# Optimization experiments

Measured on AMD Instinct MI355X. Metric: run time of the kernel, lower is better.

The kernel has to match this reference:

```python
import jax, jax.numpy as jnp
import numpy as np
from jax import lax

PAD_ID = 0
V, E = 100000, 300          # word vocab / embedding dim
VC, EC, C = 100, 50, 100    # char vocab / char emb dim / char conv channels
H, L = 256, 17              # lstm hidden / n_labels
B, S, LC = 32, 128, 50


def _conv1d(x, w, b):
    # x [B, Cin, T], w [Cout, Cin, K] -> valid conv
    y = lax.conv_general_dilated(x, w, window_strides=(1,), padding='VALID',
                                 dimension_numbers=('NCH', 'OIH', 'NCH'))
    return y + b[None, :, None]


def _lstm_dir(x_sbd, w_ih, w_hh, b, h0, c0):
    # x_sbd [S,B,D]; PyTorch gate order i,f,g,o
    def step(carry, x_t):
        h, c = carry
        g = x_t @ w_ih.T + h @ w_hh.T + b
        i, f, gg, o = jnp.split(g, 4, axis=-1)
        c = jax.nn.sigmoid(f) * c + jax.nn.sigmoid(i) * jnp.tanh(gg)
        h = jax.nn.sigmoid(o) * jnp.tanh(c)
        return (h, c), h
    _, hs = lax.scan(step, (h0, c0), x_sbd)
    return hs  # [S,B,H]


def _emissions(x, x_char, word_emb, char_emb,
               conv1_w, conv1_b, conv2_w, conv2_b, conv3_w, conv3_b,
               w_ih_f, w_hh_f, b_f, w_ih_b, w_hh_b, b_b, h0, c0, fc_w, fc_b):
    emb = word_emb[x]                                   # [B,S,E]
    ce = char_emb[x_char].transpose(0, 2, 1)            # [B,EC,LC]
    ce = jax.nn.relu(_conv1d(ce, conv1_w, conv1_b))
    ce = jax.nn.relu(_conv1d(ce, conv2_w, conv2_b))
    ce = jax.nn.relu(_conv1d(ce, conv3_w, conv3_b))
    pooled = ce.max(axis=2)                             # [B,C] (max over time)
    char_rep = jnp.broadcast_to(pooled[:, None, :], (emb.shape[0], emb.shape[1], pooled.shape[1]))
    xin = jnp.concatenate([emb, char_rep], axis=2)      # [B,S,E+C]
    xs = xin.transpose(1, 0, 2)                         # [S,B,D]
    hf = _lstm_dir(xs, w_ih_f, w_hh_f, b_f, h0[0], c0[0])
    hb = _lstm_dir(xs[::-1], w_ih_b, w_hh_b, b_b, h0[1], c0[1])[::-1]
    hcat = jnp.concatenate([hf, hb], axis=-1).transpose(1, 0, 2)  # [B,S,2H]
    em = hcat @ fc_w.T + fc_b                           # [B,S,L]
    return jax.nn.softmax(em, axis=1)                   # faithful: softmax over seq dim


def _viterbi(emissions, mask, start_t, trans, end_t):
    # emissions [B,S,L], mask [B,S]
    em = emissions.transpose(1, 0, 2)                   # [S,B,L]
    m = mask.T                                          # [S,B]
    score0 = start_t[None, :] + em[0]                   # [B,L]

    def fwd(score, inp):
        e_t, m_t = inp
        cand = score[:, :, None] + trans[None] + e_t[:, None, :]  # [B,L,L]
        nscore = cand.max(axis=1)
        idx = cand.argmax(axis=1).astype(jnp.int32)
        score = jnp.where(m_t[:, None] > 0, nscore, score)
        return score, idx

    score, hist = lax.scan(fwd, score0, (em[1:], m[1:]))  # hist [S-1,B,L]
    score = score + end_t[None, :]
    last = jnp.argmax(score, axis=-1).astype(jnp.int32)   # [B]

    def back(cur, inp):
        h_t, m_t = inp
        prev = jnp.take_along_axis(h_t, cur[:, None], axis=1)[:, 0]
        cur = jnp.where(m_t > 0, prev, cur)
        return cur, cur

    _, tags_rev = lax.scan(back, last, (hist[::-1], m[1:][::-1]))
    tags = jnp.concatenate([tags_rev[::-1], last[None]], axis=0)  # [S,B]
    return tags.T                                                 # [B,S]


def setup_inputs() -> dict:
    key = jax.random.key(0)
    ks = jax.random.split(key, 24)
    f = lambda i, shape, s=0.1: (jax.random.normal(ks[i], shape, dtype=jnp.float32) * s)
    inp = {
        'x': jax.random.randint(ks[0], (B, S), 1, V),          # no PAD -> mask all ones
        'x_char': jax.random.randint(ks[1], (B, LC), 1, VC),
        'word_emb': f(2, (V, E), 1.0),
        'char_emb': f(3, (VC, EC), 1.0).at[PAD_ID].set(0.0),
        'conv1_w': f(4, (C, EC, 3)), 'conv1_b': f(5, (C,)),
        'conv2_w': f(6, (C, C, 4)), 'conv2_b': f(7, (C,)),
        'conv3_w': f(8, (C, C, 5)), 'conv3_b': f(9, (C,)),
        'w_ih_f': f(10, (4 * H, E + C)), 'w_hh_f': f(11, (4 * H, H)), 'b_f': f(12, (4 * H,)),
        'w_ih_b': f(13, (4 * H, E + C)), 'w_hh_b': f(14, (4 * H, H)), 'b_b': f(15, (4 * H,)),
        'h0': f(16, (2, B, H), 1.0), 'c0': f(17, (2, B, H), 1.0),
        'fc_w': f(18, (L, 2 * H)), 'fc_b': f(19, (L,)),
        'start_t': f(20, (L,)), 'trans': f(21, (L, L)), 'end_t': f(22, (L,)),
    }
    return inp


def reference(x, x_char, word_emb, char_emb, conv1_w, conv1_b, conv2_w, conv2_b,
              conv3_w, conv3_b, w_ih_f, w_hh_f, b_f, w_ih_b, w_hh_b, b_b,
              h0, c0, fc_w, fc_b, start_t, trans, end_t):
    mask = (x != PAD_ID).astype(jnp.float32)
    em = _emissions(x, x_char, word_emb, char_emb, conv1_w, conv1_b, conv2_w, conv2_b,
                    conv3_w, conv3_b, w_ih_f, w_hh_f, b_f, w_ih_b, w_hh_b, b_b,
                    h0, c0, fc_w, fc_b)
    return _viterbi(em, mask, start_t, trans, end_t)
```

## Files before the change

### kernel.cpp

```cpp
#include <hip/hip_runtime.h>
#include <cmath>

#define B_   32
#define S_   128
#define E_   300
#define C_   100
#define EC_  50
#define LC_  50
#define H_   256
#define G4_  1024
#define L_   17
#define DHID_ 400
#define NBLKD 8
#define SLAB_ 8192
#define SENT2_ 0x7E007E00u
#define KP_   208

typedef _Float16 half8 __attribute__((ext_vector_type(8)));
typedef float f32x4 __attribute__((ext_vector_type(4)));
typedef unsigned long long ull;
struct __align__(16) U2 { ull x, y; };

__device__ __forceinline__ unsigned pack_split(float v) {
  _Float16 hi = (fabsf(v) >= 6.104e-5f) ? (_Float16)v : (_Float16)0.0f;
  float hif = (float)hi;
  _Float16 lo = (_Float16)((v - hif) * 2048.0f);
  return (unsigned)__builtin_bit_cast(unsigned short, hi)
       | ((unsigned)__builtin_bit_cast(unsigned short, lo) << 16);
}

__global__ void k_hinit(const float* __restrict__ h0, unsigned* __restrict__ hfrag) {
  int idx = blockIdx.x * 256 + threadIdx.x;
  const int total = 2 * (S_ + 1) * SLAB_;
  if (idx >= total) return;
  int sd = idx / SLAB_;
  int within = idx % SLAB_;
  int t = sd % (S_ + 1), d = sd / (S_ + 1);
  if (t != 0) { hfrag[idx] = SENT2_; return; }
  int m8 = within & 7;
  int lane = (within >> 3) & 63;
  int q = within >> 9;
  int Kt = q & 7, Nt = q >> 3;
  int m = m8 & 3, isLo = m8 >> 2;
  int k0 = Kt * 32 + (lane >> 4) * 8 + 2 * m;
  int b = Nt * 16 + (lane & 15);
  unsigned p0 = pack_split(h0[((size_t)d * B_ + b) * H_ + k0]);
  unsigned p1 = pack_split(h0[((size_t)d * B_ + b) * H_ + k0 + 1]);
  unsigned hiw = (p0 & 0xFFFFu) | (p1 << 16);
  unsigned low = (p0 >> 16) | (p1 & 0xFFFF0000u);
  hfrag[idx] = isLo ? low : hiw;
}

__global__ void k_conv1(const int* __restrict__ x_char, const float* __restrict__ char_emb,
                        const float* __restrict__ w1, const float* __restrict__ b1,
                        float* __restrict__ out1) {
  int b = blockIdx.x;
  int ot = blockIdx.y;
  __shared__ float ce[EC_ * 52];
  __shared__ float wl[50 * 150];
  __shared__ int ids[LC_];
  int tid = threadIdx.x;
  if (tid < LC_) ids[tid] = x_char[b * LC_ + tid];
  __syncthreads();
  for (int idx = tid; idx < LC_ * EC_; idx += 256) {
    int t = idx / EC_, ec = idx % EC_;
    ce[ec * 52 + t] = char_emb[ids[t] * EC_ + ec];
  }
  int obase = ot * 50;
  for (int idx = tid; idx < 50 * 150; idx += 256)
    wl[idx] = w1[obase * 150 + idx];
  __syncthreads();
  for (int idx = tid; idx < 50 * 48; idx += 256) {
    int o = idx / 48, t = idx % 48;
    float acc = b1[obase + o];
    const float* wr = &wl[o * 150];
    for (int c = 0; c < EC_; ++c) {
      const float* ip = &ce[c * 52 + t];
      acc += wr[c * 3 + 0] * ip[0] + wr[c * 3 + 1] * ip[1] + wr[c * 3 + 2] * ip[2];
    }
    out1[((size_t)b * C_ + obase + o) * 48 + t] = fmaxf(acc, 0.0f);
  }
}

__global__ void k_conv2(const float* __restrict__ in, const float* __restrict__ w2,
                        const float* __restrict__ b2, float* __restrict__ out2) {
  int b = blockIdx.x, ot = blockIdx.y;
  __shared__ float il[C_ * 48];
  __shared__ float wl[25 * 400];
  int tid = threadIdx.x;
  for (int idx = tid; idx < C_ * 48; idx += 256) il[idx] = in[(size_t)b * C_ * 48 + idx];
  int obase = ot * 25;
  for (int idx = tid; idx < 25 * 400; idx += 256) wl[idx] = w2[obase * 400 + idx];
  __syncthreads();
  for (int idx = tid; idx < 25 * 45; idx += 256) {
    int o = idx / 45, t = idx % 45;
    float acc = b2[obase + o];
    const float* wr = &wl[o * 400];
    for (int c = 0; c < C_; ++c) {
      const float* ip = &il[c * 48 + t];
      acc += wr[c * 4 + 0] * ip[0] + wr[c * 4 + 1] * ip[1] +
             wr[c * 4 + 2] * ip[2] + wr[c * 4 + 3] * ip[3];
    }
    out2[((size_t)b * C_ + obase + o) * 45 + t] = fmaxf(acc, 0.0f);
  }
}

__global__ void k_conv3(const float* __restrict__ in, const float* __restrict__ w3,
                        const float* __restrict__ b3, float* __restrict__ pooled) {
  int b = blockIdx.x, ot = blockIdx.y;
  __shared__ float il[C_ * 45];
  __shared__ float wl[20 * 500];
  __shared__ float o3[20 * 44];
  int tid = threadIdx.x;
  for (int idx = tid; idx < C_ * 45; idx += 256) il[idx] = in[(size_t)b * C_ * 45 + idx];
  int obase = ot * 20;
  for (int idx = tid; idx < 20 * 500; idx += 256) wl[idx] = w3[obase * 500 + idx];
  __syncthreads();
  for (int idx = tid; idx < 20 * 41; idx += 256) {
    int o = idx / 41, t = idx % 41;
    float acc = b3[obase + o];
    const float* wr = &wl[o * 500];
    for (int c = 0; c < C_; ++c) {
      const float* ip = &il[c * 45 + t];
      acc += wr[c * 5 + 0] * ip[0] + wr[c * 5 + 1] * ip[1] + wr[c * 5 + 2] * ip[2] +
             wr[c * 5 + 3] * ip[3] + wr[c * 5 + 4] * ip[4];
    }
    o3[o * 44 + t] = fmaxf(acc, 0.0f);
  }
  __syncthreads();
  if (tid < 20) {
    float m = o3[tid * 44];
    for (int t = 1; t < 41; ++t) m = fmaxf(m, o3[tid * 44 + t]);
    pooled[b * C_ + obase + tid] = m;
  }
}

__global__ void k_prep_w(const float* __restrict__ wf, const float* __restrict__ wb,
                         unsigned* __restrict__ apH, unsigned* __restrict__ apL) {
  int idx = blockIdx.x * 256 + threadIdx.x;
  if (idx >= 2 * G4_ * KP_) return;
  int d = idx / (G4_ * KP_);
  int rem = idx % (G4_ * KP_);
  int j = rem / KP_, k2 = rem % KP_;
  const float* w = d ? wb : wf;
  float v0 = 0.f, v1 = 0.f;
  if (k2 < 200) { v0 = w[(size_t)j * DHID_ + 2 * k2]; v1 = w[(size_t)j * DHID_ + 2 * k2 + 1]; }
  unsigned p0 = pack_split(v0), p1 = pack_split(v1);
  apH[idx] = (p0 & 0xFFFFu) | (p1 << 16);
  apL[idx] = (p0 >> 16) | (p1 & 0xFFFF0000u);
}

__global__ void k_prep_b(const int* __restrict__ x, const float* __restrict__ word_emb,
                         const float* __restrict__ pooled,
                         unsigned* __restrict__ bpH, unsigned* __restrict__ bpL) {
  int r = blockIdx.x;
  int k2 = threadIdx.x;
  if (k2 >= KP_) return;
  int t = r >> 5, b = r & 31;
  float v0 = 0.f, v1 = 0.f;
  if (k2 < 150) {
    const float* e = word_emb + (size_t)x[b * S_ + t] * E_;
    v0 = e[2 * k2]; v1 = e[2 * k2 + 1];
  } else if (k2 < 200) {
    v0 = pooled[b * C_ + 2 * k2 - 300];
    v1 = pooled[b * C_ + 2 * k2 - 299];
  }
  unsigned p0 = pack_split(v0), p1 = pack_split(v1);
  bpH[(size_t)r * KP_ + k2] = (p0 & 0xFFFFu) | (p1 << 16);
  bpL[(size_t)r * KP_ + k2] = (p0 >> 16) | (p1 & 0xFFFF0000u);
}

__global__ __launch_bounds__(256) void k_gemm(
    const unsigned* __restrict__ apH, const unsigned* __restrict__ apL,
    const unsigned* __restrict__ bpH, const unsigned* __restrict__ bpL,
    const float* __restrict__ b_f, const float* __restrict__ b_b,
    float* __restrict__ gi) {
  const int jt = blockIdx.x, rt = blockIdx.y, d = blockIdx.z;
  const int j0 = jt * 128, r0 = rt * 128;
  const int tid = threadIdx.x;
  const int w = tid >> 6, l = tid & 63;
  const int lx = l & 15, lq = l >> 4;

  __shared__ unsigned aH[2048], aL[2048], bH[2048], bL[2048];

  f32x4 acch[2][8], accl[2][8];
#pragma unroll
  for (int mt = 0; mt < 2; ++mt)
#pragma unroll
    for (int nt = 0; nt < 8; ++nt) {
      f32x4 z = {0.f, 0.f, 0.f, 0.f};
      acch[mt][nt] = z; accl[mt][nt] = z;
    }

  const int jr = tid >> 1, hh = tid & 1;
  const int q_st = jr >> 4, lane_lo = jr & 15;
  const unsigned* arH = apH + ((size_t)(d * G4_ + j0 + jr)) * KP_ + hh * 8;
  const unsigned* arL = apL + ((size_t)(d * G4_ + j0 + jr)) * KP_ + hh * 8;
  const unsigned* brH = bpH + ((size_t)(r0 + jr)) * KP_ + hh * 8;
  const unsigned* brL = bpL + ((size_t)(r0 + jr)) * KP_ + hh * 8;
  const int w0 = (q_st * 64 + lane_lo + 32 * hh) * 4;
  const int w1 = (q_st * 64 + lane_lo + 32 * hh + 16) * 4;

  for (int Kt = 0; Kt < 13; ++Kt) {
    uint4 a0 = *(const uint4*)(arH + Kt * 16);
    uint4 a1 = *(const uint4*)(arH + Kt * 16 + 4);
    uint4 c0 = *(const uint4*)(arL + Kt * 16);
    uint4 c1 = *(const uint4*)(arL + Kt * 16 + 4);
    uint4 e0 = *(const uint4*)(brH + Kt * 16);
    uint4 e1 = *(const uint4*)(brH + Kt * 16 + 4);
    uint4 f0 = *(const uint4*)(brL + Kt * 16);
    uint4 f1 = *(const uint4*)(brL + Kt * 16 + 4);
    *(uint4*)&aH[w0] = a0; *(uint4*)&aH[w1] = a1;
    *(uint4*)&aL[w0] = c0; *(uint4*)&aL[w1] = c1;
    *(uint4*)&bH[w0] = e0; *(uint4*)&bH[w1] = e1;
    *(uint4*)&bL[w0] = f0; *(uint4*)&bL[w1] = f1;
    __syncthreads();

    union u4h { uint4 u; half8 h; };
    u4h AH0, AH1, AL0, AL1;
    AH0.u = *(const uint4*)&aH[((2 * w + 0) * 64 + l) * 4];
    AH1.u = *(const uint4*)&aH[((2 * w + 1) * 64 + l) * 4];
    AL0.u = *(const uint4*)&aL[((2 * w + 0) * 64 + l) * 4];
    AL1.u = *(const uint4*)&aL[((2 * w + 1) * 64 + l) * 4];
#pragma unroll
    for (int nt = 0; nt < 8; ++nt) {
      u4h BHn, BLn;
      BHn.u = *(const uint4*)&bH[(nt * 64 + l) * 4];
      BLn.u = *(const uint4*)&bL[(nt * 64 + l) * 4];
      acch[0][nt] = __builtin_amdgcn_mfma_f32_16x16x32_f16(AH0.h, BHn.h, acch[0][nt], 0, 0, 0);
      accl[0][nt] = __builtin_amdgcn_mfma_f32_16x16x32_f16(AH0.h, BLn.h, accl[0][nt], 0, 0, 0);
      accl[0][nt] = __builtin_amdgcn_mfma_f32_16x16x32_f16(AL0.h, BHn.h, accl[0][nt], 0, 0, 0);
      acch[1][nt] = __builtin_amdgcn_mfma_f32_16x16x32_f16(AH1.h, BHn.h, acch[1][nt], 0, 0, 0);
      accl[1][nt] = __builtin_amdgcn_mfma_f32_16x16x32_f16(AH1.h, BLn.h, accl[1][nt], 0, 0, 0);
      accl[1][nt] = __builtin_amdgcn_mfma_f32_16x16x32_f16(AL1.h, BHn.h, accl[1][nt], 0, 0, 0);
    }
    __syncthreads();
  }

  const float* bias = d ? b_b : b_f;
  const float inv2048 = 1.0f / 2048.0f;
#pragma unroll
  for (int mt = 0; mt < 2; ++mt) {
#pragma unroll
    for (int nt = 0; nt < 8; ++nt) {
      int rr = r0 + nt * 16 + lx;
      int tt = rr >> 5, bb = rr & 31;
      float* dst = gi + ((size_t)(d * S_ + tt) * G4_) * B_ + bb;
#pragma unroll
      for (int r4 = 0; r4 < 4; ++r4) {
        int j = j0 + (2 * w + mt) * 16 + lq * 4 + r4;
        dst[(size_t)j * B_] = acch[mt][nt][r4] + accl[mt][nt][r4] * inv2048 + bias[j];
      }
    }
  }
}

__global__ __launch_bounds__(256, 1) void k_lstm(
    const float* __restrict__ w_hh_f, const float* __restrict__ w_hh_b,
    const float* __restrict__ c0, const float* __restrict__ gi,
    float* __restrict__ hbuf, unsigned* __restrict__ hfrag) {
  const int iblk = blockIdx.x;
  const int d = blockIdx.y;
  const float* whh = d ? w_hh_b : w_hh_f;
  const int tid = threadIdx.x;
  const int w = tid >> 6;
  const int l = tid & 63;
  const int lx = l & 15, lq = l >> 4;
  const int u0 = iblk * 32;

  __shared__ ull slh[2048];
  __shared__ ull sll[2048];
  __shared__ float gl[4 * 32 * 33];
  __shared__ unsigned ps[2 * 576];

  half8 whi[2][8], wlo[2][8];
#pragma unroll
  for (int Mt = 0; Mt < 2; ++Mt) {
#pragma unroll
    for (int Kt = 0; Kt < 8; ++Kt) {
      int row = w * H_ + u0 + Mt * 16 + lx;
      int kk0 = Kt * 32 + lq * 8;
      const float* src = whh + (size_t)row * H_ + kk0;
      float4 f0 = *(const float4*)src;
      float4 f1 = *(const float4*)(src + 4);
      float wv[8] = {f0.x, f0.y, f0.z, f0.w, f1.x, f1.y, f1.z, f1.w};
      union { unsigned short s[8]; half8 h; } HI, LO;
#pragma unroll
      for (int j = 0; j < 8; ++j) {
        float v = wv[j];
        _Float16 hi = (fabsf(v) >= 6.104e-5f) ? (_Float16)v : (_Float16)0.0f;
        float hif = (float)hi;
        _Float16 lo = (_Float16)((v - hif) * 2048.0f);
        HI.s[j] = __builtin_bit_cast(unsigned short, hi);
        LO.s[j] = __builtin_bit_cast(unsigned short, lo);
      }
      whi[Mt][Kt] = HI.h;
      wlo[Mt][Kt] = LO.h;
    }
  }

  const int bc = tid & 31, cw = tid >> 5;
  float creg[4];
#pragma unroll
  for (int cu = 0; cu < 4; ++cu)
    creg[cu] = c0[((size_t)d * B_ + bc) * H_ + u0 + cu * 8 + cw];

  const int pNt = bc >> 4;
  const int pm = cw >> 1;
  const bool phi = (cw & 1) == 0;
  const int plane = bc & 15;
  const float inv2048 = 1.0f / 2048.0f;

  for (int t = 0; t < S_; ++t) {
    int torig = d ? (S_ - 1 - t) : t;

    f32x4 acch[2][2], accl[2][2];
    {
      const float* gbase = gi + ((size_t)(d * S_ + torig) * G4_) * B_;
#pragma unroll
      for (int Mt = 0; Mt < 2; ++Mt)
#pragma unroll
        for (int Nt = 0; Nt < 2; ++Nt) {
          f32x4 v;
#pragma unroll
          for (int r = 0; r < 4; ++r) {
            int j = w * H_ + u0 + Mt * 16 + lq * 4 + r;
            v[r] = gbase[(size_t)j * B_ + Nt * 16 + lx];
          }
          acch[Mt][Nt] = v;
          f32x4 z = {0.f, 0.f, 0.f, 0.f};
          accl[Mt][Nt] = z;
        }
    }

    const ull* hp = (const ull*)(hfrag + (size_t)(d * (S_ + 1) + t) * SLAB_);
    ull pv[4][4];
#pragma unroll
    for (int c = 0; c < 4; ++c) {
      size_t base = ((size_t)(w * 4 + c) * 64 + l) * 4;
#pragma unroll
      for (int j = 0; j < 4; ++j)
        pv[c][j] = __hip_atomic_load(&hp[base + j], __ATOMIC_RELAXED,
                                     __HIP_MEMORY_SCOPE_AGENT);
    }
    for (;;) {
      bool pending = false;
#pragma unroll
      for (int c = 0; c < 4; ++c)
#pragma unroll
        for (int j = 0; j < 4; ++j)
          pending |= ((unsigned)pv[c][j] == SENT2_) |
                     ((unsigned)(pv[c][j] >> 32) == SENT2_);
      if (!pending) break;
#pragma unroll
      for (int c = 0; c < 4; ++c) {
        size_t base = ((size_t)(w * 4 + c) * 64 + l) * 4;
#pragma unroll
        for (int j = 0; j < 4; ++j)
          pv[c][j] = __hip_atomic_load(&hp[base + j], __ATOMIC_RELAXED,
                                       __HIP_MEMORY_SCOPE_AGENT);
      }
    }
#pragma unroll
    for (int c = 0; c < 4; ++c) {
      int idx = ((w * 4 + c) * 64 + l) * 2;
      U2 vh; vh.x = pv[c][0]; vh.y = pv[c][1];
      U2 vl; vl.x = pv[c][2]; vl.y = pv[c][3];
      *(U2*)&slh[idx] = vh;
      *(U2*)&sll[idx] = vl;
    }
    __syncthreads();

#pragma unroll
    for (int Kt = 0; Kt < 8; ++Kt) {
      half8 Bhi[2], Blo[2];
#pragma unroll
      for (int Nt = 0; Nt < 2; ++Nt) {
        int idx = ((Nt * 8 + Kt) * 64 + l) * 2;
        union { U2 u; half8 h; } UH, UL;
        UH.u = *(const U2*)&slh[idx];
        UL.u = *(const U2*)&sll[idx];
        Bhi[Nt] = UH.h;
        Blo[Nt] = UL.h;
      }
#pragma unroll
      for (int Mt = 0; Mt < 2; ++Mt)
#pragma unroll
        for (int Nt = 0; Nt < 2; ++Nt) {
          acch[Mt][Nt] = __builtin_amdgcn_mfma_f32_16x16x32_f16(
              whi[Mt][Kt], Bhi[Nt], acch[Mt][Nt], 0, 0, 0);
          accl[Mt][Nt] = __builtin_amdgcn_mfma_f32_16x16x32_f16(
              whi[Mt][Kt], Blo[Nt], accl[Mt][Nt], 0, 0, 0);
          accl[Mt][Nt] = __builtin_amdgcn_mfma_f32_16x16x32_f16(
              wlo[Mt][Kt], Bhi[Nt], accl[Mt][Nt], 0, 0, 0);
        }
    }

#pragma unroll
    for (int Mt = 0; Mt < 2; ++Mt)
#pragma unroll
      for (int Nt = 0; Nt < 2; ++Nt)
#pragma unroll
        for (int r = 0; r < 4; ++r) {
          int ul = Mt * 16 + lq * 4 + r;
          gl[(w * 32 + ul) * 33 + Nt * 16 + lx] =
              acch[Mt][Nt][r] + accl[Mt][Nt][r] * inv2048;
        }
    __syncthreads();

    float hreg[4];
#pragma unroll
    for (int cu = 0; cu < 4; ++cu) {
      int u = cu * 8 + cw;
      float g_i = gl[(0 * 32 + u) * 33 + bc];
      float g_f = gl[(1 * 32 + u) * 33 + bc];
      float g_g = gl[(2 * 32 + u) * 33 + bc];
      float g_o = gl[(3 * 32 + u) * 33 + bc];
      float si = 1.f / (1.f + __expf(-g_i));
      float sf = 1.f / (1.f + __expf(-g_f));
      float so = 1.f / (1.f + __expf(-g_o));
      float tg = 1.f - 2.f / (__expf(2.f * g_g) + 1.f);
      float cn = sf * creg[cu] + si * tg;
      float tc = 1.f - 2.f / (__expf(2.f * cn) + 1.f);
      float hn = so * tc;
      creg[cu] = cn;
      hreg[cu] = hn;
      unsigned me = pack_split(hn);
      unsigned pa = (unsigned)__shfl_xor((int)me, 32, 64);
      unsigned je = (cw & 1) ? pa : me;
      unsigned jo = (cw & 1) ? me : pa;
      unsigned hiw = (je & 0xFFFFu) | (jo << 16);
      unsigned low = (je >> 16) | (jo & 0xFFFF0000u);
      int lane2 = (cu << 4) | plane;
      int m8 = phi ? pm : (4 + pm);
      ps[pNt * 576 + lane2 * 9 + m8] = phi ? hiw : low;
    }
    __syncthreads();

    {
      ull* slab64 = (ull*)(hfrag + (size_t)(d * (S_ + 1) + t + 1) * SLAB_);
#pragma unroll
      for (int hh2 = 0; hh2 < 2; ++hh2) {
        int r = tid;
        int Nt = hh2;
        int lane2 = r >> 2, m2 = r & 3;
        unsigned a = ps[Nt * 576 + lane2 * 9 + 2 * m2];
        unsigned b = ps[Nt * 576 + lane2 * 9 + 2 * m2 + 1];
        ull v = (ull)a | ((ull)b << 32);
        __hip_atomic_store(&slab64[(size_t)(Nt * 8 + iblk) * 256 + r], v,
                           __ATOMIC_RELAXED, __HIP_MEMORY_SCOPE_AGENT);
      }
      float* hb = hbuf + (size_t)(d * (S_ + 1) + t + 1) * (H_ * B_) + u0 * B_;
#pragma unroll
      for (int cu = 0; cu < 4; ++cu) hb[cu * 256 + tid] = hreg[cu];
    }
  }
}

__global__ __launch_bounds__(256) void k_fc(const float* __restrict__ hbuf,
                                            const float* __restrict__ fc_w,
                                            const float* __restrict__ fc_b,
                                            float* __restrict__ em) {
  const int s = blockIdx.x;
  const int tid = threadIdx.x;
  __shared__ float wT[512 * 18];
  __shared__ float psum[256 * 18];
  for (int i = tid; i < L_ * 512; i += 256) {
    int l = i / 512, k = i % 512;
    wT[k * 18 + l] = fc_w[i];
  }
  __syncthreads();
  const int b = tid & 31, kq = tid >> 5;
  const float* hf = hbuf + (size_t)(s + 1) * (H_ * B_);
  const float* hbk = hbuf + (size_t)(S_ + 1 + (S_ - s)) * (H_ * B_);
  float acc[L_];
#pragma unroll
  for (int l = 0; l < L_; ++l) acc[l] = 0.f;
  for (int i = 0; i < 64; ++i) {
    int k = kq * 64 + i;
    float hv = (k < 256) ? hf[k * 32 + b] : hbk[(k - 256) * 32 + b];
    const float* wr = &wT[k * 18];
#pragma unroll
    for (int l = 0; l < L_; ++l) acc[l] = fmaf(hv, wr[l], acc[l]);
  }
#pragma unroll
  for (int l = 0; l < L_; ++l) psum[tid * 18 + l] = acc[l];
  __syncthreads();
  for (int idx = tid; idx < B_ * L_; idx += 256) {
    int bb = idx & 31, l = idx >> 5;
    float sum = fc_b[l];
    for (int q = 0; q < 8; ++q) sum += psum[(q * 32 + bb) * 18 + l];
    em[((size_t)bb * S_ + s) * L_ + l] = sum;
  }
}

__global__ void k_smv(const float* __restrict__ em, const int* __restrict__ x,
                      const float* __restrict__ start_t, const float* __restrict__ trans,
                      const float* __restrict__ end_t, int* __restrict__ out) {
  int b = blockIdx.x;
  int tid = threadIdx.x;
  __shared__ float e[S_ * L_];
  __shared__ float tr[L_ * L_];
  __shared__ float sc[2][L_];
  __shared__ int hist[(S_ - 1) * L_];
  __shared__ int tags[S_];
  for (int i = tid; i < S_ * L_; i += 64) e[i] = em[(size_t)b * S_ * L_ + i];
  for (int i = tid; i < L_ * L_; i += 64) tr[i] = trans[i];
  __syncthreads();
  if (tid < L_) {
    int l = tid;
    float m = -INFINITY;
    for (int s = 0; s < S_; ++s) m = fmaxf(m, e[s * L_ + l]);
    float sum = 0.f;
    for (int s = 0; s < S_; ++s) {
      float ex = expf(e[s * L_ + l] - m);
      e[s * L_ + l] = ex;
      sum += ex;
    }
    for (int s = 0; s < S_; ++s) e[s * L_ + l] = e[s * L_ + l] / sum;
  }
  __syncthreads();
  if (tid < L_) sc[0][tid] = start_t[tid] + e[tid];
  __syncthreads();
  int cbuf = 0;
  for (int t = 1; t < S_; ++t) {
    if (tid < L_) {
      int j = tid;
      float ev = e[t * L_ + j];
      float best = -INFINITY;
      int arg = 0;
      for (int i = 0; i < L_; ++i) {
        float v = (sc[cbuf][i] + tr[i * L_ + j]) + ev;
        if (v > best) { best = v; arg = i; }
      }
      int maskt = (x[b * S_ + t] != 0);
      sc[cbuf ^ 1][j] = maskt ? best : sc[cbuf][j];
      hist[(t - 1) * L_ + j] = arg;
    }
    __syncthreads();
    cbuf ^= 1;
  }
  if (tid == 0) {
    float best = -INFINITY;
    int last = 0;
    for (int j = 0; j < L_; ++j) {
      float v = sc[cbuf][j] + end_t[j];
      if (v > best) { best = v; last = j; }
    }
    int cur = last;
    tags[S_ - 1] = cur;
    for (int p = S_ - 2; p >= 0; --p) {
      if (x[b * S_ + p + 1] != 0) cur = hist[p * L_ + cur];
      tags[p] = cur;
    }
  }
  __syncthreads();
  for (int s = tid; s < S_; s += 64) out[b * S_ + s] = tags[s];
}

extern "C" void kernel_launch(void* const* d_in, const int* in_sizes, int n_in,
                              void* d_out, int out_size, void* d_ws, size_t ws_size,
                              hipStream_t stream) {
  const int* x        = (const int*)d_in[0];
  const int* x_char   = (const int*)d_in[1];
  const float* word_emb = (const float*)d_in[2];
  const float* char_emb = (const float*)d_in[3];
  const float* conv1_w = (const float*)d_in[4];
  const float* conv1_b = (const float*)d_in[5];
  const float* conv2_w = (const float*)d_in[6];
  const float* conv2_b = (const float*)d_in[7];
  const float* conv3_w = (const float*)d_in[8];
  const float* conv3_b = (const float*)d_in[9];
  const float* w_ih_f = (const float*)d_in[10];
  const float* w_hh_f = (const float*)d_in[11];
  const float* b_f    = (const float*)d_in[12];
  const float* w_ih_b = (const float*)d_in[13];
  const float* w_hh_b = (const float*)d_in[14];
  const float* b_b    = (const float*)d_in[15];
  const float* h0     = (const float*)d_in[16];
  const float* c0     = (const float*)d_in[17];
  const float* fc_w   = (const float*)d_in[18];
  const float* fc_b   = (const float*)d_in[19];
  const float* start_t = (const float*)d_in[20];
  const float* trans  = (const float*)d_in[21];
  const float* end_t  = (const float*)d_in[22];
  int* out = (int*)d_out;

  char* ws = (char*)d_ws;
  auto alloc = [&](size_t bytes) -> char* {
    char* p = ws;
    ws += (bytes + 1023) & ~(size_t)1023;
    return p;
  };
  float* pooled  = (float*)alloc(sizeof(float) * B_ * C_);
  float* gi      = (float*)alloc(sizeof(float) * 2 * S_ * G4_ * B_);
  float* hbuf    = (float*)alloc(sizeof(float) * 2 * (S_ + 1) * H_ * B_);
  unsigned* hfrag = (unsigned*)alloc(sizeof(unsigned) * 2 * (S_ + 1) * SLAB_);
  unsigned* apH  = (unsigned*)alloc(sizeof(unsigned) * 2 * G4_ * KP_);
  unsigned* apL  = (unsigned*)alloc(sizeof(unsigned) * 2 * G4_ * KP_);
  unsigned* bpH  = (unsigned*)alloc(sizeof(unsigned) * 4096 * KP_);
  unsigned* bpL  = (unsigned*)alloc(sizeof(unsigned) * 4096 * KP_);
  float* out1    = (float*)alloc(sizeof(float) * B_ * C_ * 48);
  float* out2    = (float*)alloc(sizeof(float) * B_ * C_ * 45);
  float* em      = (float*)alloc(sizeof(float) * B_ * S_ * L_);

  const int hinit_total = 2 * (S_ + 1) * SLAB_;
  k_hinit<<<(hinit_total + 255) / 256, 256, 0, stream>>>(h0, hfrag);
  k_prep_w<<<(2 * G4_ * KP_ + 255) / 256, 256, 0, stream>>>(w_ih_f, w_ih_b, apH, apL);
  k_conv1<<<dim3(32, 2), 256, 0, stream>>>(x_char, char_emb, conv1_w, conv1_b, out1);
  k_conv2<<<dim3(32, 4), 256, 0, stream>>>(out1, conv2_w, conv2_b, out2);
  k_conv3<<<dim3(32, 5), 256, 0, stream>>>(out2, conv3_w, conv3_b, pooled);
  k_prep_b<<<4096, 256, 0, stream>>>(x, word_emb, pooled, bpH, bpL);
  k_gemm<<<dim3(8, 32, 2), 256, 0, stream>>>(apH, apL, bpH, bpL, b_f, b_b, gi);
  k_lstm<<<dim3(NBLKD, 2), 256, 0, stream>>>(w_hh_f, w_hh_b, c0, gi, hbuf, hfrag);
  k_fc<<<S_, 256, 0, stream>>>(hbuf, fc_w, fc_b, em);
  k_smv<<<B_, 64, 0, stream>>>(em, x, start_t, trans, end_t, out);
}
```

Baseline: 930.2 us.

## Fuse all stages into one persistent megakernel with flag and sentinel dataflow sync

Replaces the ten-kernel launch sequence with a fill kernel plus one megakernel. Its blocks are partitioned by role: LSTM, convs, prep, GEMM, FC and Viterbi. Stages synchronise through atomic counters and NaN-sentinel polling on gi, hbuf and em, so the FC and Viterbi stages can overlap the LSTM recurrence and launch gaps disappear. The cost is filling large sentinel buffers and spin-waiting, plus a deadlock risk if producer blocks are not co-resident with the consumers that wait on them.

```diff
diff --git a/kernel.cpp b/kernel.cpp
--- a/kernel.cpp
+++ b/kernel.cpp
@@ -14,7 +14,34 @@
 #define NBLKD 8
 #define SLAB_ 8192
 #define SENT2_ 0x7E007E00u
+#define SENTF_ 0x7FC0DEADu
 #define KP_   208
+
+#define RB_LSTM 0
+#define NB_LSTM 16
+#define RB_C1   16
+#define NB_C1   64
+#define RB_C2   80
+#define NB_C2   128
+#define RB_C3   208
+#define NB_C3   160
+#define RB_PW   368
+#define NB_PW   64
+#define RB_PB   432
+#define NB_PB   512
+#define RB_GEMM 944
+#define NB_GEMM 512
+#define RB_FC   1456
+#define NB_FC   128
+#define RB_SMV  1584
+#define NB_SMV  32
+#define NBLK_MEGA 1616
+
+#define F_C1 0
+#define F_C2 1
+#define F_C3 2
+#define F_PW 3
+#define F_PB 4
 
 typedef _Float16 half8 __attribute__((ext_vector_type(8)));
 typedef float f32x4 __attribute__((ext_vector_type(4)));
@@ -29,329 +56,159 @@
        | ((unsigned)__builtin_bit_cast(unsigned short, lo) << 16);
 }
 
-__global__ void k_hinit(const float* __restrict__ h0, unsigned* __restrict__ hfrag) {
-  int idx = blockIdx.x * 256 + threadIdx.x;
-  const int total = 2 * (S_ + 1) * SLAB_;
-  if (idx >= total) return;
-  int sd = idx / SLAB_;
-  int within = idx % SLAB_;
-  int t = sd % (S_ + 1), d = sd / (S_ + 1);
-  if (t != 0) { hfrag[idx] = SENT2_; return; }
-  int m8 = within & 7;
-  int lane = (within >> 3) & 63;
-  int q = within >> 9;
-  int Kt = q & 7, Nt = q >> 3;
-  int m = m8 & 3, isLo = m8 >> 2;
-  int k0 = Kt * 32 + (lane >> 4) * 8 + 2 * m;
-  int b = Nt * 16 + (lane & 15);
-  unsigned p0 = pack_split(h0[((size_t)d * B_ + b) * H_ + k0]);
-  unsigned p1 = pack_split(h0[((size_t)d * B_ + b) * H_ + k0 + 1]);
-  unsigned hiw = (p0 & 0xFFFFu) | (p1 << 16);
-  unsigned low = (p0 >> 16) | (p1 & 0xFFFF0000u);
-  hfrag[idx] = isLo ? low : hiw;
+__device__ __forceinline__ void flag_signal(int* f) {
+  __syncthreads();
+  if (threadIdx.x == 0)
+    __hip_atomic_fetch_add(f, 1, __ATOMIC_RELEASE, __HIP_MEMORY_SCOPE_AGENT);
 }
-
-__global__ void k_conv1(const int* __restrict__ x_char, const float* __restrict__ char_emb,
-                        const float* __restrict__ w1, const float* __restrict__ b1,
-                        float* __restrict__ out1) {
-  int b = blockIdx.x;
-  int ot = blockIdx.y;
-  __shared__ float ce[EC_ * 52];
-  __shared__ float wl[50 * 150];
-  __shared__ int ids[LC_];
-  int tid = threadIdx.x;
-  if (tid < LC_) ids[tid] = x_char[b * LC_ + tid];
-  __syncthreads();
-  for (int idx = tid; idx < LC_ * EC_; idx += 256) {
-    int t = idx / EC_, ec = idx % EC_;
-    ce[ec * 52 + t] = char_emb[ids[t] * EC_ + ec];
-  }
-  int obase = ot * 50;
-  for (int idx = tid; idx < 50 * 150; idx += 256)
-    wl[idx] = w1[obase * 150 + idx];
-  __syncthreads();
-  for (int idx = tid; idx < 50 * 48; idx += 256) {
-    int o = idx / 48, t = idx % 48;
-    float acc = b1[obase + o];
-    const float* wr = &wl[o * 150];
-    for (int c = 0; c < EC_; ++c) {
-      const float* ip = &ce[c * 52 + t];
-      acc += wr[c * 3 + 0] * ip[0] + wr[c * 3 + 1] * ip[1] + wr[c * 3 + 2] * ip[2];
-    }
-    out1[((size_t)b * C_ + obase + o) * 48 + t] = fmaxf(acc, 0.0f);
+__device__ __forceinline__ void flag_wait(const int* f, int target, int slp) {
+  while (__hip_atomic_load(f, __ATOMIC_ACQUIRE, __HIP_MEMORY_SCOPE_AGENT) < target) {
+    switch (slp) {
+      case 4:  __builtin_amdgcn_s_sleep(4);  break;
+      case 8:  __builtin_amdgcn_s_sleep(8);  break;
+      default: __builtin_amdgcn_s_sleep(16); break;
+    }
   }
 }
 
-__global__ void k_conv2(const float* __restrict__ in, const float* __restrict__ w2,
-                        const float* __restrict__ b2, float* __restrict__ out2) {
-  int b = blockIdx.x, ot = blockIdx.y;
-  __shared__ float il[C_ * 48];
-  __shared__ float wl[25 * 400];
-  int tid = threadIdx.x;
-  for (int idx = tid; idx < C_ * 48; idx += 256) il[idx] = in[(size_t)b * C_ * 48 + idx];
-  int obase = ot * 25;
-  for (int idx = tid; idx < 25 * 400; idx += 256) wl[idx] = w2[obase * 400 + idx];
-  __syncthreads();
-  for (int idx = tid; idx < 25 * 45; idx += 256) {
-    int o = idx / 45, t = idx % 45;
-    float acc = b2[obase + o];
-    const float* wr = &wl[o * 400];
-    for (int c = 0; c < C_; ++c) {
-      const float* ip = &il[c * 48 + t];
-      acc += wr[c * 4 + 0] * ip[0] + wr[c * 4 + 1] * ip[1] +
-             wr[c * 4 + 2] * ip[2] + wr[c * 4 + 3] * ip[3];
-    }
-    out2[((size_t)b * C_ + obase + o) * 45 + t] = fmaxf(acc, 0.0f);
-  }
+union SMem {
+  struct { unsigned aH[2048], aL[2048], bH[2048], bL[2048]; } gemm;
+  struct { ull slh[2048], sll[2048]; float gl[4 * 32 * 33]; unsigned ps[2 * 576]; } lstm;
+  struct { float ce[EC_ * 52]; float wl[50 * 150]; int ids[LC_]; } c1;
+  struct { float il[C_ * 48]; float wl[25 * 400]; } c2;
+  struct { float il[C_ * 45]; float wl[20 * 500]; float o3[20 * 44]; } c3;
+  struct { float wT[512 * 18]; float psum[256 * 18]; } fc;
+  struct { float e[S_ * L_]; float tr[L_ * L_]; float sc[2][L_];
+           int hist[(S_ - 1) * L_]; int tags[S_]; } smv;
+};
+
+__global__ void k_fill(const float* __restrict__ h0, unsigned* __restrict__ hfrag,
+                       unsigned* __restrict__ hbufU, unsigned* __restrict__ giU,
+                       unsigned* __restrict__ emU, int* __restrict__ flags) {
+  const int g0 = blockIdx.x * 256 + threadIdx.x;
+  const int nth = gridDim.x * 256;
+  const int htot = 2 * (S_ + 1) * SLAB_;
+  for (int idx = g0; idx < htot; idx += nth) {
+    int sd = idx / SLAB_;
+    int within = idx % SLAB_;
+    int t = sd % (S_ + 1), d = sd / (S_ + 1);
+    if (t != 0) { hfrag[idx] = SENT2_; continue; }
+    int m8 = within & 7;
+    int lane = (within >> 3) & 63;
+    int q = within >> 9;
+    int Kt = q & 7, Nt = q >> 3;
+    int m = m8 & 3, isLo = m8 >> 2;
+    int k0 = Kt * 32 + (lane >> 4) * 8 + 2 * m;
+    int b = Nt * 16 + (lane & 15);
+    unsigned p0 = pack_split(h0[((size_t)d * B_ + b) * H_ + k0]);
+    unsigned p1 = pack_split(h0[((size_t)d * B_ + b) * H_ + k0 + 1]);
+    unsigned hiw = (p0 & 0xFFFFu) | (p1 << 16);
+    unsigned low = (p0 >> 16) | (p1 & 0xFFFF0000u);
+    hfrag[idx] = isLo ? low : hiw;
+  }
+  const int hbtot = 2 * (S_ + 1) * H_ * B_;
+  for (int idx = g0; idx < hbtot; idx += nth) hbufU[idx] = SENTF_;
+  const int gtot = 2 * S_ * G4_ * B_;
+  for (int idx = g0; idx < gtot; idx += nth) giU[idx] = SENTF_;
+  const int etot = B_ * S_ * L_;
+  for (int idx = g0; idx < etot; idx += nth) emU[idx] = SENTF_;
+  if (g0 < 16) flags[g0] = 0;
 }
 
-__global__ void k_conv3(const float* __restrict__ in, const float* __restrict__ w3,
-                        const float* __restrict__ b3, float* __restrict__ pooled) {
-  int b = blockIdx.x, ot = blockIdx.y;
-  __shared__ float il[C_ * 45];
-  __shared__ float wl[20 * 500];
-  __shared__ float o3[20 * 44];
-  int tid = threadIdx.x;
-  for (int idx = tid; idx < C_ * 45; idx += 256) il[idx] = in[(size_t)b * C_ * 45 + idx];
-  int obase = ot * 20;
-  for (int idx = tid; idx < 20 * 500; idx += 256) wl[idx] = w3[obase * 500 + idx];
-  __syncthreads();
-  for (int idx = tid; idx < 20 * 41; idx += 256) {
-    int o = idx / 41, t = idx % 41;
-    float acc = b3[obase + o];
-    const float* wr = &wl[o * 500];
-    for (int c = 0; c < C_; ++c) {
-      const float* ip = &il[c * 45 + t];
-      acc += wr[c * 5 + 0] * ip[0] + wr[c * 5 + 1] * ip[1] + wr[c * 5 + 2] * ip[2] +
-             wr[c * 5 + 3] * ip[3] + wr[c * 5 + 4] * ip[4];
-    }
-    o3[o * 44 + t] = fmaxf(acc, 0.0f);
-  }
-  __syncthreads();
-  if (tid < 20) {
-    float m = o3[tid * 44];
-    for (int t = 1; t < 41; ++t) m = fmaxf(m, o3[tid * 44 + t]);
-    pooled[b * C_ + obase + tid] = m;
-  }
-}
-
-__global__ void k_prep_w(const float* __restrict__ wf, const float* __restrict__ wb,
-                         unsigned* __restrict__ apH, unsigned* __restrict__ apL) {
-  int idx = blockIdx.x * 256 + threadIdx.x;
-  if (idx >= 2 * G4_ * KP_) return;
-  int d = idx / (G4_ * KP_);
-  int rem = idx % (G4_ * KP_);
-  int j = rem / KP_, k2 = rem % KP_;
-  const float* w = d ? wb : wf;
-  float v0 = 0.f, v1 = 0.f;
-  if (k2 < 200) { v0 = w[(size_t)j * DHID_ + 2 * k2]; v1 = w[(size_t)j * DHID_ + 2 * k2 + 1]; }
-  unsigned p0 = pack_split(v0), p1 = pack_split(v1);
-  apH[idx] = (p0 & 0xFFFFu) | (p1 << 16);
-  apL[idx] = (p0 >> 16) | (p1 & 0xFFFF0000u);
-}
-
-__global__ void k_prep_b(const int* __restrict__ x, const float* __restrict__ word_emb,
-                         const float* __restrict__ pooled,
-                         unsigned* __restrict__ bpH, unsigned* __restrict__ bpL) {
-  int r = blockIdx.x;
-  int k2 = threadIdx.x;
-  if (k2 >= KP_) return;
-  int t = r >> 5, b = r & 31;
-  float v0 = 0.f, v1 = 0.f;
-  if (k2 < 150) {
-    const float* e = word_emb + (size_t)x[b * S_ + t] * E_;
-    v0 = e[2 * k2]; v1 = e[2 * k2 + 1];
-  } else if (k2 < 200) {
-    v0 = pooled[b * C_ + 2 * k2 - 300];
-    v1 = pooled[b * C_ + 2 * k2 - 299];
-  }
-  unsigned p0 = pack_split(v0), p1 = pack_split(v1);
-  bpH[(size_t)r * KP_ + k2] = (p0 & 0xFFFFu) | (p1 << 16);
-  bpL[(size_t)r * KP_ + k2] = (p0 >> 16) | (p1 & 0xFFFF0000u);
-}
-
-__global__ __launch_bounds__(256) void k_gemm(
-    const unsigned* __restrict__ apH, const unsigned* __restrict__ apL,
-    const unsigned* __restrict__ bpH, const unsigned* __restrict__ bpL,
+__global__ __launch_bounds__(256, 2) void k_mega(
+    const int* __restrict__ x, const int* __restrict__ x_char,
+    const float* __restrict__ word_emb, const float* __restrict__ char_emb,
+    const float* __restrict__ conv1_w, const float* __restrict__ conv1_b,
+    const float* __restrict__ conv2_w, const float* __restrict__ conv2_b,
+    const float* __restrict__ conv3_w, const float* __restrict__ conv3_b,
+    const float* __restrict__ w_ih_f, const float* __restrict__ w_ih_b,
+    const float* __restrict__ w_hh_f, const float* __restrict__ w_hh_b,
     const float* __restrict__ b_f, const float* __restrict__ b_b,
-    float* __restrict__ gi) {
-  const int jt = blockIdx.x, rt = blockIdx.y, d = blockIdx.z;
-  const int j0 = jt * 128, r0 = rt * 128;
-  const int tid = threadIdx.x;
-  const int w = tid >> 6, l = tid & 63;
-  const int lx = l & 15, lq = l >> 4;
-
-  __shared__ unsigned aH[2048], aL[2048], bH[2048], bL[2048];
-
-  f32x4 acch[2][8], accl[2][8];
-#pragma unroll
-  for (int mt = 0; mt < 2; ++mt)
-#pragma unroll
-    for (int nt = 0; nt < 8; ++nt) {
-      f32x4 z = {0.f, 0.f, 0.f, 0.f};
-      acch[mt][nt] = z; accl[mt][nt] = z;
-    }
-
-  const int jr = tid >> 1, hh = tid & 1;
-  const int q_st = jr >> 4, lane_lo = jr & 15;
-  const unsigned* arH = apH + ((size_t)(d * G4_ + j0 + jr)) * KP_ + hh * 8;
-  const unsigned* arL = apL + ((size_t)(d * G4_ + j0 + jr)) * KP_ + hh * 8;
-  const unsigned* brH = bpH + ((size_t)(r0 + jr)) * KP_ + hh * 8;
-  const unsigned* brL = bpL + ((size_t)(r0 + jr)) * KP_ + hh * 8;
-  const int w0 = (q_st * 64 + lane_lo + 32 * hh) * 4;
-  const int w1 = (q_st * 64 + lane_lo + 32 * hh + 16) * 4;
-
-  for (int Kt = 0; Kt < 13; ++Kt) {
-    uint4 a0 = *(const uint4*)(arH + Kt * 16);
-    uint4 a1 = *(const uint4*)(arH + Kt * 16 + 4);
-    uint4 c0 = *(const uint4*)(arL + Kt * 16);
-    uint4 c1 = *(const uint4*)(arL + Kt * 16 + 4);
-    uint4 e0 = *(const uint4*)(brH + Kt * 16);
-    uint4 e1 = *(const uint4*)(brH + Kt * 16 + 4);
-    uint4 f0 = *(const uint4*)(brL + Kt * 16);
-    uint4 f1 = *(const uint4*)(brL + Kt * 16 + 4);
-    *(uint4*)&aH[w0] = a0; *(uint4*)&aH[w1] = a1;
-    *(uint4*)&aL[w0] = c0; *(uint4*)&aL[w1] = c1;
-    *(uint4*)&bH[w0] = e0; *(uint4*)&bH[w1] = e1;
-    *(uint4*)&bL[w0] = f0; *(uint4*)&bL[w1] = f1;
-    __syncthreads();
-
-    union u4h { uint4 u; half8 h; };
-    u4h AH0, AH1, AL0, AL1;
-    AH0.u = *(const uint4*)&aH[((2 * w + 0) * 64 + l) * 4];
-    AH1.u = *(const uint4*)&aH[((2 * w + 1) * 64 + l) * 4];
-    AL0.u = *(const uint4*)&aL[((2 * w + 0) * 64 + l) * 4];
-    AL1.u = *(const uint4*)&aL[((2 * w + 1) * 64 + l) * 4];
-#pragma unroll
-    for (int nt = 0; nt < 8; ++nt) {
-      u4h BHn, BLn;
-      BHn.u = *(const uint4*)&bH[(nt * 64 + l) * 4];
-      BLn.u = *(const uint4*)&bL[(nt * 64 + l) * 4];
-      acch[0][nt] = __builtin_amdgcn_mfma_f32_16x16x32_f16(AH0.h, BHn.h, acch[0][nt], 0, 0, 0);
-      accl[0][nt] = __builtin_amdgcn_mfma_f32_16x16x32_f16(AH0.h, BLn.h, accl[0][nt], 0, 0, 0);
-      accl[0][nt] = __builtin_amdgcn_mfma_f32_16x16x32_f16(AL0.h, BHn.h, accl[0][nt], 0, 0, 0);
-      acch[1][nt] = __builtin_amdgcn_mfma_f32_16x16x32_f16(AH1.h, BHn.h, acch[1][nt], 0, 0, 0);
-      accl[1][nt] = __builtin_amdgcn_mfma_f32_16x16x32_f16(AH1.h, BLn.h, accl[1][nt], 0, 0, 0);
-      accl[1][nt] = __builtin_amdgcn_mfma_f32_16x16x32_f16(AL1.h, BHn.h, accl[1][nt], 0, 0, 0);
-    }
-    __syncthreads();
-  }
-
-  const float* bias = d ? b_b : b_f;
-  const float inv2048 = 1.0f / 2048.0f;
-#pragma unroll
-  for (int mt = 0; mt < 2; ++mt) {
-#pragma unroll
-    for (int nt = 0; nt < 8; ++nt) {
-      int rr = r0 + nt * 16 + lx;
-      int tt = rr >> 5, bb = rr & 31;
-      float* dst = gi + ((size_t)(d * S_ + tt) * G4_) * B_ + bb;
-#pragma unroll
-      for (int r4 = 0; r4 < 4; ++r4) {
-        int j = j0 + (2 * w + mt) * 16 + lq * 4 + r4;
-        dst[(size_t)j * B_] = acch[mt][nt][r4] + accl[mt][nt][r4] * inv2048 + bias[j];
-      }
-    }
-  }
-}
-
-__global__ __launch_bounds__(256, 1) void k_lstm(
-    const float* __restrict__ w_hh_f, const float* __restrict__ w_hh_b,
-    const float* __restrict__ c0, const float* __restrict__ gi,
-    float* __restrict__ hbuf, unsigned* __restrict__ hfrag) {
-  const int iblk = blockIdx.x;
-  const int d = blockIdx.y;
-  const float* whh = d ? w_hh_b : w_hh_f;
-  const int tid = threadIdx.x;
-  const int w = tid >> 6;
-  const int l = tid & 63;
-  const int lx = l & 15, lq = l >> 4;
-  const int u0 = iblk * 32;
-
-  __shared__ ull slh[2048];
-  __shared__ ull sll[2048];
-  __shared__ float gl[4 * 32 * 33];
-  __shared__ unsigned ps[2 * 576];
-
-  half8 whi[2][8], wlo[2][8];
-#pragma unroll
-  for (int Mt = 0; Mt < 2; ++Mt) {
-#pragma unroll
-    for (int Kt = 0; Kt < 8; ++Kt) {
-      int row = w * H_ + u0 + Mt * 16 + lx;
-      int kk0 = Kt * 32 + lq * 8;
-      const float* src = whh + (size_t)row * H_ + kk0;
-      float4 f0 = *(const float4*)src;
-      float4 f1 = *(const float4*)(src + 4);
-      float wv[8] = {f0.x, f0.y, f0.z, f0.w, f1.x, f1.y, f1.z, f1.w};
-      union { unsigned short s[8]; half8 h; } HI, LO;
-#pragma unroll
-      for (int j = 0; j < 8; ++j) {
-        float v = wv[j];
-        _Float16 hi = (fabsf(v) >= 6.104e-5f) ? (_Float16)v : (_Float16)0.0f;
-        float hif = (float)hi;
-        _Float16 lo = (_Float16)((v - hif) * 2048.0f);
-        HI.s[j] = __builtin_bit_cast(unsigned short, hi);
-        LO.s[j] = __builtin_bit_cast(unsigned short, lo);
-      }
-      whi[Mt][Kt] = HI.h;
-      wlo[Mt][Kt] = LO.h;
-    }
-  }
-
-  const int bc = tid & 31, cw = tid >> 5;
-  float creg[4];
-#pragma unroll
-  for (int cu = 0; cu < 4; ++cu)
-    creg[cu] = c0[((size_t)d * B_ + bc) * H_ + u0 + cu * 8 + cw];
-
-  const int pNt = bc >> 4;
-  const int pm = cw >> 1;
-  const bool phi = (cw & 1) == 0;
-  const int plane = bc & 15;
-  const float inv2048 = 1.0f / 2048.0f;
-
-  for (int t = 0; t < S_; ++t) {
-    int torig = d ? (S_ - 1 - t) : t;
-
-    f32x4 acch[2][2], accl[2][2];
-    {
-      const float* gbase = gi + ((size_t)(d * S_ + torig) * G4_) * B_;
+    const float* __restrict__ c0,
+    const float* __restrict__ fc_w, const float* __restrict__ fc_b,
+    const float* __restrict__ start_t, const float* __restrict__ trans,
+    const float* __restrict__ end_t,
+    float* __restrict__ pooled, float* __restrict__ gi, float* __restrict__ hbuf,
+    unsigned* __restrict__ hfrag,
+    unsigned* __restrict__ apH, unsigned* __restrict__ apL,
+    unsigned* __restrict__ bpH, unsigned* __restrict__ bpL,
+    float* __restrict__ out1, float* __restrict__ out2,
+    float* __restrict__ em, int* __restrict__ flags, int* __restrict__ out) {
+  const int bid = blockIdx.x;
+  __shared__ SMem sm;
+
+  if (bid < RB_C1) {
+    __builtin_amdgcn_s_setprio(2);
+    const int iblk = bid & 7;
+    const int d = bid >> 3;
+    const float* whh = d ? w_hh_b : w_hh_f;
+    const int tid = threadIdx.x;
+    const int w = tid >> 6;
+    const int l = tid & 63;
+    const int lx = l & 15, lq = l >> 4;
+    const int u0 = iblk * 32;
+
+    ull* slh = sm.lstm.slh;
+    ull* sll = sm.lstm.sll;
+    float* glb = sm.lstm.gl;
+    unsigned* ps = sm.lstm.ps;
+
+    half8 whi[2][8], wlo[2][8];
+#pragma unroll
+    for (int Mt = 0; Mt < 2; ++Mt) {
+#pragma unroll
+      for (int Kt = 0; Kt < 8; ++Kt) {
+        int row = w * H_ + u0 + Mt * 16 + lx;
+        int kk0 = Kt * 32 + lq * 8;
+        const float* src = whh + (size_t)row * H_ + kk0;
+        float4 f0 = *(const float4*)src;
+        float4 f1 = *(const float4*)(src + 4);
+        float wv[8] = {f0.x, f0.y, f0.z, f0.w, f1.x, f1.y, f1.z, f1.w};
+        union { unsigned short s2[8]; half8 h; } HI, LO;
+#pragma unroll
+        for (int j = 0; j < 8; ++j) {
+          float v = wv[j];
+          _Float16 hi = (fabsf(v) >= 6.104e-5f) ? (_Float16)v : (_Float16)0.0f;
+          float hif = (float)hi;
+          _Float16 lo = (_Float16)((v - hif) * 2048.0f);
+          HI.s2[j] = __builtin_bit_cast(unsigned short, hi);
+          LO.s2[j] = __builtin_bit_cast(unsigned short, lo);
+        }
+        whi[Mt][Kt] = HI.h;
+        wlo[Mt][Kt] = LO.h;
+      }
+    }
+
+    const int bc = tid & 31, cw = tid >> 5;
+    float creg[4];
+#pragma unroll
+    for (int cu = 0; cu < 4; ++cu)
+      creg[cu] = c0[((size_t)d * B_ + bc) * H_ + u0 + cu * 8 + cw];
+
+    const int pNt = bc >> 4;
+    const int pm = cw >> 1;
+    const bool phi = (cw & 1) == 0;
+    const int plane = bc & 15;
+    const float inv2048 = 1.0f / 2048.0f;
+
+    for (int t = 0; t < S_; ++t) {
+      int torig = d ? (S_ - 1 - t) : t;
+
+      const unsigned* gbase = (const unsigned*)gi + ((size_t)(d * S_ + torig) * G4_) * B_;
+      unsigned gv[2][2][4];
 #pragma unroll
       for (int Mt = 0; Mt < 2; ++Mt)
 #pragma unroll
-        for (int Nt = 0; Nt < 2; ++Nt) {
-          f32x4 v;
+        for (int Nt = 0; Nt < 2; ++Nt)
 #pragma unroll
           for (int r = 0; r < 4; ++r) {
             int j = w * H_ + u0 + Mt * 16 + lq * 4 + r;
-            v[r] = gbase[(size_t)j * B_ + Nt * 16 + lx];
+            gv[Mt][Nt][r] = __hip_atomic_load(&gbase[(size_t)j * B_ + Nt * 16 + lx],
+                                              __ATOMIC_RELAXED, __HIP_MEMORY_SCOPE_AGENT);
           }
-          acch[Mt][Nt] = v;
-          f32x4 z = {0.f, 0.f, 0.f, 0.f};
-          accl[Mt][Nt] = z;
-        }
-    }
-
-    const ull* hp = (const ull*)(hfrag + (size_t)(d * (S_ + 1) + t) * SLAB_);
-    ull pv[4][4];
-#pragma unroll
-    for (int c = 0; c < 4; ++c) {
-      size_t base = ((size_t)(w * 4 + c) * 64 + l) * 4;
-#pragma unroll
-      for (int j = 0; j < 4; ++j)
-        pv[c][j] = __hip_atomic_load(&hp[base + j], __ATOMIC_RELAXED,
-                                     __HIP_MEMORY_SCOPE_AGENT);
-    }
-    for (;;) {
-      bool pending = false;
-#pragma unroll
-      for (int c = 0; c < 4; ++c)
-#pragma unroll
-        for (int j = 0; j < 4; ++j)
-          pending |= ((unsigned)pv[c][j] == SENT2_) |
-                     ((unsigned)(pv[c][j] >> 32) == SENT2_);
-      if (!pending) break;
+
+      const ull* hp = (const ull*)(hfrag + (size_t)(d * (S_ + 1) + t) * SLAB_);
+      ull pv[4][4];
 #pragma unroll
       for (int c = 0; c < 4; ++c) {
         size_t base = ((size_t)(w * 4 + c) * 64 + l) * 4;
@@ -360,202 +217,523 @@
           pv[c][j] = __hip_atomic_load(&hp[base + j], __ATOMIC_RELAXED,
                                        __HIP_MEMORY_SCOPE_AGENT);
       }
-    }
-#pragma unroll
-    for (int c = 0; c < 4; ++c) {
-      int idx = ((w * 4 + c) * 64 + l) * 2;
-      U2 vh; vh.x = pv[c][0]; vh.y = pv[c][1];
-      U2 vl; vl.x = pv[c][2]; vl.y = pv[c][3];
-      *(U2*)&slh[idx] = vh;
-      *(U2*)&sll[idx] = vl;
-    }
-    __syncthreads();
-
-#pragma unroll
-    for (int Kt = 0; Kt < 8; ++Kt) {
-      half8 Bhi[2], Blo[2];
-#pragma unroll
-      for (int Nt = 0; Nt < 2; ++Nt) {
-        int idx = ((Nt * 8 + Kt) * 64 + l) * 2;
-        union { U2 u; half8 h; } UH, UL;
-        UH.u = *(const U2*)&slh[idx];
-        UL.u = *(const U2*)&sll[idx];
-        Bhi[Nt] = UH.h;
-        Blo[Nt] = UL.h;
-      }
+      for (;;) {
+        bool pending = false;
+#pragma unroll
+        for (int c = 0; c < 4; ++c)
+#pragma unroll
+          for (int j = 0; j < 4; ++j)
+            pending |= ((unsigned)pv[c][j] == SENT2_) |
+                       ((unsigned)(pv[c][j] >> 32) == SENT2_);
+        if (!pending) break;
+#pragma unroll
+        for (int c = 0; c < 4; ++c) {
+          size_t base = ((size_t)(w * 4 + c) * 64 + l) * 4;
+#pragma unroll
+          for (int j = 0; j < 4; ++j)
+            pv[c][j] = __hip_atomic_load(&hp[base + j], __ATOMIC_RELAXED,
+                                         __HIP_MEMORY_SCOPE_AGENT);
+        }
+      }
+
+      for (;;) {
+        bool pending = false;
+#pragma unroll
+        for (int Mt = 0; Mt < 2; ++Mt)
+#pragma unroll
+          for (int Nt = 0; Nt < 2; ++Nt)
+#pragma unroll
+            for (int r = 0; r < 4; ++r) pending |= (gv[Mt][Nt][r] == SENTF_);
+        if (!pending) break;
+#pragma unroll
+        for (int Mt = 0; Mt < 2; ++Mt)
+#pragma unroll
+          for (int Nt = 0; Nt < 2; ++Nt)
+#pragma unroll
+            for (int r = 0; r < 4; ++r) {
+              int j = w * H_ + u0 + Mt * 16 + lq * 4 + r;
+              gv[Mt][Nt][r] = __hip_atomic_load(&gbase[(size_t)j * B_ + Nt * 16 + lx],
+                                                __ATOMIC_RELAXED, __HIP_MEMORY_SCOPE_AGENT);
+            }
+      }
+
+      f32x4 acch[2][2], accl[2][2];
 #pragma unroll
       for (int Mt = 0; Mt < 2; ++Mt)
 #pragma unroll
         for (int Nt = 0; Nt < 2; ++Nt) {
-          acch[Mt][Nt] = __builtin_amdgcn_mfma_f32_16x16x32_f16(
-              whi[Mt][Kt], Bhi[Nt], acch[Mt][Nt], 0, 0, 0);
-          accl[Mt][Nt] = __builtin_amdgcn_mfma_f32_16x16x32_f16(
-              whi[Mt][Kt], Blo[Nt], accl[Mt][Nt], 0, 0, 0);
-          accl[Mt][Nt] = __builtin_amdgcn_mfma_f32_16x16x32_f16(
-              wlo[Mt][Kt], Bhi[Nt], accl[Mt][Nt], 0, 0, 0);
+          f32x4 v, z = {0.f, 0.f, 0.f, 0.f};
+#pragma unroll
+          for (int r = 0; r < 4; ++r) v[r] = __builtin_bit_cast(float, gv[Mt][Nt][r]);
+          acch[Mt][Nt] = v;
+          accl[Mt][Nt] = z;
         }
-    }
-
-#pragma unroll
-    for (int Mt = 0; Mt < 2; ++Mt)
-#pragma unroll
-      for (int Nt = 0; Nt < 2; ++Nt)
-#pragma unroll
-        for (int r = 0; r < 4; ++r) {
-          int ul = Mt * 16 + lq * 4 + r;
-          gl[(w * 32 + ul) * 33 + Nt * 16 + lx] =
-              acch[Mt][Nt][r] + accl[Mt][Nt][r] * inv2048;
+
+#pragma unroll
+      for (int c = 0; c < 4; ++c) {
+        int idx = ((w * 4 + c) * 64 + l) * 2;
+        U2 vh; vh.x = pv[c][0]; vh.y = pv[c][1];
+        U2 vl; vl.x = pv[c][2]; vl.y = pv[c][3];
+        *(U2*)&slh[idx] = vh;
+        *(U2*)&sll[idx] = vl;
+      }
+      __syncthreads();
+
+#pragma unroll
+      for (int Kt = 0; Kt < 8; ++Kt) {
+        half8 Bhi[2], Blo[2];
+#pragma unroll
+        for (int Nt = 0; Nt < 2; ++Nt) {
+          int idx = ((Nt * 8 + Kt) * 64 + l) * 2;
+          union { U2 u; half8 h; } UH, UL;
+          UH.u = *(const U2*)&slh[idx];
+          UL.u = *(const U2*)&sll[idx];
+          Bhi[Nt] = UH.h;
+          Blo[Nt] = UL.h;
         }
-    __syncthreads();
-
-    float hreg[4];
-#pragma unroll
-    for (int cu = 0; cu < 4; ++cu) {
-      int u = cu * 8 + cw;
-      float g_i = gl[(0 * 32 + u) * 33 + bc];
-      float g_f = gl[(1 * 32 + u) * 33 + bc];
-      float g_g = gl[(2 * 32 + u) * 33 + bc];
-      float g_o = gl[(3 * 32 + u) * 33 + bc];
-      float si = 1.f / (1.f + __expf(-g_i));
-      float sf = 1.f / (1.f + __expf(-g_f));
-      float so = 1.f / (1.f + __expf(-g_o));
-      float tg = 1.f - 2.f / (__expf(2.f * g_g) + 1.f);
-      float cn = sf * creg[cu] + si * tg;
-      float tc = 1.f - 2.f / (__expf(2.f * cn) + 1.f);
-      float hn = so * tc;
-      creg[cu] = cn;
-      hreg[cu] = hn;
-      unsigned me = pack_split(hn);
-      unsigned pa = (unsigned)__shfl_xor((int)me, 32, 64);
-      unsigned je = (cw & 1) ? pa : me;
-      unsigned jo = (cw & 1) ? me : pa;
-      unsigned hiw = (je & 0xFFFFu) | (jo << 16);
-      unsigned low = (je >> 16) | (jo & 0xFFFF0000u);
-      int lane2 = (cu << 4) | plane;
-      int m8 = phi ? pm : (4 + pm);
-      ps[pNt * 576 + lane2 * 9 + m8] = phi ? hiw : low;
-    }
-    __syncthreads();
-
-    {
-      ull* slab64 = (ull*)(hfrag + (size_t)(d * (S_ + 1) + t + 1) * SLAB_);
-#pragma unroll
-      for (int hh2 = 0; hh2 < 2; ++hh2) {
-        int r = tid;
-        int Nt = hh2;
-        int lane2 = r >> 2, m2 = r & 3;
-        unsigned a = ps[Nt * 576 + lane2 * 9 + 2 * m2];
-        unsigned b = ps[Nt * 576 + lane2 * 9 + 2 * m2 + 1];
-        ull v = (ull)a | ((ull)b << 32);
-        __hip_atomic_store(&slab64[(size_t)(Nt * 8 + iblk) * 256 + r], v,
-                           __ATOMIC_RELAXED, __HIP_MEMORY_SCOPE_AGENT);
-      }
-      float* hb = hbuf + (size_t)(d * (S_ + 1) + t + 1) * (H_ * B_) + u0 * B_;
-#pragma unroll
-      for (int cu = 0; cu < 4; ++cu) hb[cu * 256 + tid] = hreg[cu];
-    }
-  }
-}
-
-__global__ __launch_bounds__(256) void k_fc(const float* __restrict__ hbuf,
-                                            const float* __restrict__ fc_w,
-                                            const float* __restrict__ fc_b,
-                                            float* __restrict__ em) {
-  const int s = blockIdx.x;
-  const int tid = threadIdx.x;
-  __shared__ float wT[512 * 18];
-  __shared__ float psum[256 * 18];
-  for (int i = tid; i < L_ * 512; i += 256) {
-    int l = i / 512, k = i % 512;
-    wT[k * 18 + l] = fc_w[i];
-  }
-  __syncthreads();
-  const int b = tid & 31, kq = tid >> 5;
-  const float* hf = hbuf + (size_t)(s + 1) * (H_ * B_);
-  const float* hbk = hbuf + (size_t)(S_ + 1 + (S_ - s)) * (H_ * B_);
-  float acc[L_];
-#pragma unroll
-  for (int l = 0; l < L_; ++l) acc[l] = 0.f;
-  for (int i = 0; i < 64; ++i) {
-    int k = kq * 64 + i;
-    float hv = (k < 256) ? hf[k * 32 + b] : hbk[(k - 256) * 32 + b];
-    const float* wr = &wT[k * 18];
-#pragma unroll
-    for (int l = 0; l < L_; ++l) acc[l] = fmaf(hv, wr[l], acc[l]);
-  }
-#pragma unroll
-  for (int l = 0; l < L_; ++l) psum[tid * 18 + l] = acc[l];
-  __syncthreads();
-  for (int idx = tid; idx < B_ * L_; idx += 256) {
-    int bb = idx & 31, l = idx >> 5;
-    float sum = fc_b[l];
-    for (int q = 0; q < 8; ++q) sum += psum[(q * 32 + bb) * 18 + l];
-    em[((size_t)bb * S_ + s) * L_ + l] = sum;
-  }
-}
-
-__global__ void k_smv(const float* __restrict__ em, const int* __restrict__ x,
-                      const float* __restrict__ start_t, const float* __restrict__ trans,
-                      const float* __restrict__ end_t, int* __restrict__ out) {
-  int b = blockIdx.x;
-  int tid = threadIdx.x;
-  __shared__ float e[S_ * L_];
-  __shared__ float tr[L_ * L_];
-  __shared__ float sc[2][L_];
-  __shared__ int hist[(S_ - 1) * L_];
-  __shared__ int tags[S_];
-  for (int i = tid; i < S_ * L_; i += 64) e[i] = em[(size_t)b * S_ * L_ + i];
-  for (int i = tid; i < L_ * L_; i += 64) tr[i] = trans[i];
-  __syncthreads();
-  if (tid < L_) {
-    int l = tid;
-    float m = -INFINITY;
-    for (int s = 0; s < S_; ++s) m = fmaxf(m, e[s * L_ + l]);
-    float sum = 0.f;
-    for (int s = 0; s < S_; ++s) {
-      float ex = expf(e[s * L_ + l] - m);
-      e[s * L_ + l] = ex;
-      sum += ex;
-    }
-    for (int s = 0; s < S_; ++s) e[s * L_ + l] = e[s * L_ + l] / sum;
-  }
-  __syncthreads();
-  if (tid < L_) sc[0][tid] = start_t[tid] + e[tid];
-  __syncthreads();
-  int cbuf = 0;
-  for (int t = 1; t < S_; ++t) {
+#pragma unroll
+        for (int Mt = 0; Mt < 2; ++Mt)
+#pragma unroll
+          for (int Nt = 0; Nt < 2; ++Nt) {
+            acch[Mt][Nt] = __builtin_amdgcn_mfma_f32_16x16x32_f16(
+                whi[Mt][Kt], Bhi[Nt], acch[Mt][Nt], 0, 0, 0);
+            accl[Mt][Nt] = __builtin_amdgcn_mfma_f32_16x16x32_f16(
+                whi[Mt][Kt], Blo[Nt], accl[Mt][Nt], 0, 0, 0);
+            accl[Mt][Nt] = __builtin_amdgcn_mfma_f32_16x16x32_f16(
+                wlo[Mt][Kt], Bhi[Nt], accl[Mt][Nt], 0, 0, 0);
+          }
+      }
+
+#pragma unroll
+      for (int Mt = 0; Mt < 2; ++Mt)
+#pragma unroll
+        for (int Nt = 0; Nt < 2; ++Nt)
+#pragma unroll
+          for (int r = 0; r < 4; ++r) {
+            int ul = Mt * 16 + lq * 4 + r;
+            glb[(w * 32 + ul) * 33 + Nt * 16 + lx] =
+                acch[Mt][Nt][r] + accl[Mt][Nt][r] * inv2048;
+          }
+      __syncthreads();
+
+      float hreg[4];
+#pragma unroll
+      for (int cu = 0; cu < 4; ++cu) {
+        int u = cu * 8 + cw;
+        float g_i = glb[(0 * 32 + u) * 33 + bc];
+        float g_f = glb[(1 * 32 + u) * 33 + bc];
+        float g_g = glb[(2 * 32 + u) * 33 + bc];
+        float g_o = glb[(3 * 32 + u) * 33 + bc];
+        float si = 1.f / (1.f + __expf(-g_i));
+        float sf = 1.f / (1.f + __expf(-g_f));
+        float so = 1.f / (1.f + __expf(-g_o));
+        float tg = 1.f - 2.f / (__expf(2.f * g_g) + 1.f);
+        float cn = sf * creg[cu] + si * tg;
+        float tc = 1.f - 2.f / (__expf(2.f * cn) + 1.f);
+        float hn = so * tc;
+        creg[cu] = cn;
+        hreg[cu] = hn;
+        unsigned me = pack_split(hn);
+        unsigned pa = (unsigned)__shfl_xor((int)me, 32, 64);
+        unsigned je = (cw & 1) ? pa : me;
+        unsigned jo = (cw & 1) ? me : pa;
+        unsigned hiw = (je & 0xFFFFu) | (jo << 16);
+        unsigned low = (je >> 16) | (jo & 0xFFFF0000u);
+        int lane2 = (cu << 4) | plane;
+        int m8 = phi ? pm : (4 + pm);
+        ps[pNt * 576 + lane2 * 9 + m8] = phi ? hiw : low;
+      }
+      __syncthreads();
+
+      {
+        ull* slab64 = (ull*)(hfrag + (size_t)(d * (S_ + 1) + t + 1) * SLAB_);
+#pragma unroll
+        for (int hh2 = 0; hh2 < 2; ++hh2) {
+          int r = tid;
+          int Nt = hh2;
+          int lane2 = r >> 2, m2 = r & 3;
+          unsigned a = ps[Nt * 576 + lane2 * 9 + 2 * m2];
+          unsigned b2 = ps[Nt * 576 + lane2 * 9 + 2 * m2 + 1];
+          ull v = (ull)a | ((ull)b2 << 32);
+          __hip_atomic_store(&slab64[(size_t)(Nt * 8 + iblk) * 256 + r], v,
+                             __ATOMIC_RELAXED, __HIP_MEMORY_SCOPE_AGENT);
+        }
+        float* hb = hbuf + (size_t)(d * (S_ + 1) + t + 1) * (H_ * B_) + u0 * B_;
+#pragma unroll
+        for (int cu = 0; cu < 4; ++cu)
+          __hip_atomic_store(&hb[cu * 256 + tid], hreg[cu],
+                             __ATOMIC_RELAXED, __HIP_MEMORY_SCOPE_AGENT);
+      }
+    }
+    return;
+  }
+
+  else if (bid < RB_C2) {
+    const int q = bid - RB_C1;
+    const int b2 = q & 31, ot = q >> 5;
+    float* ce = sm.c1.ce;
+    float* wl = sm.c1.wl;
+    int* ids = sm.c1.ids;
+    const int tid = threadIdx.x;
+    if (tid < LC_) ids[tid] = x_char[b2 * LC_ + tid];
+    __syncthreads();
+    for (int idx = tid; idx < LC_ * EC_; idx += 256) {
+      int t2 = idx / EC_, ec = idx % EC_;
+      ce[ec * 52 + t2] = char_emb[ids[t2] * EC_ + ec];
+    }
+    int obase = ot * 50;
+    for (int idx = tid; idx < 50 * 150; idx += 256)
+      wl[idx] = conv1_w[obase * 150 + idx];
+    __syncthreads();
+    for (int idx = tid; idx < 50 * 48; idx += 256) {
+      int o = idx / 48, t2 = idx % 48;
+      float acc = conv1_b[obase + o];
+      const float* wr = &wl[o * 150];
+      for (int c = 0; c < EC_; ++c) {
+        const float* ip = &ce[c * 52 + t2];
+        acc += wr[c * 3 + 0] * ip[0] + wr[c * 3 + 1] * ip[1] + wr[c * 3 + 2] * ip[2];
+      }
+      out1[((size_t)b2 * C_ + obase + o) * 48 + t2] = fmaxf(acc, 0.0f);
+    }
+    flag_signal(&flags[F_C1]);
+    return;
+  }
+
+  else if (bid < RB_C3) {
+    flag_wait(&flags[F_C1], NB_C1, 4);
+    const int q = bid - RB_C2;
+    const int b2 = q & 31, ot = q >> 5;
+    float* il = sm.c2.il;
+    float* wl = sm.c2.wl;
+    const int tid = threadIdx.x;
+    for (int idx = tid; idx < C_ * 48; idx += 256) il[idx] = out1[(size_t)b2 * C_ * 48 + idx];
+    int obase = ot * 25;
+    for (int idx = tid; idx < 25 * 400; idx += 256) wl[idx] = conv2_w[obase * 400 + idx];
+    __syncthreads();
+    for (int idx = tid; idx < 25 * 45; idx += 256) {
+      int o = idx / 45, t2 = idx % 45;
+      float acc = conv2_b[obase + o];
+      const float* wr = &wl[o * 400];
+      for (int c = 0; c < C_; ++c) {
+        const float* ip = &il[c * 48 + t2];
+        acc += wr[c * 4 + 0] * ip[0] + wr[c * 4 + 1] * ip[1] +
+               wr[c * 4 + 2] * ip[2] + wr[c * 4 + 3] * ip[3];
+      }
+      out2[((size_t)b2 * C_ + obase + o) * 45 + t2] = fmaxf(acc, 0.0f);
+    }
+    flag_signal(&flags[F_C2]);
+    return;
+  }
+
+  else if (bid < RB_PW) {
+    flag_wait(&flags[F_C2], NB_C2, 4);
+    const int q = bid - RB_C3;
+    const int b2 = q % 32, ot = q / 32;
+    float* il = sm.c3.il;
+    float* wl = sm.c3.wl;
+    float* o3 = sm.c3.o3;
+    const int tid = threadIdx.x;
+    for (int idx = tid; idx < C_ * 45; idx += 256) il[idx] = out2[(size_t)b2 * C_ * 45 + idx];
+    int obase = ot * 20;
+    for (int idx = tid; idx < 20 * 500; idx += 256) wl[idx] = conv3_w[obase * 500 + idx];
+    __syncthreads();
+    for (int idx = tid; idx < 20 * 41; idx += 256) {
+      int o = idx / 41, t2 = idx % 41;
+      float acc = conv3_b[obase + o];
+      const float* wr = &wl[o * 500];
+      for (int c = 0; c < C_; ++c) {
+        const float* ip = &il[c * 45 + t2];
+        acc += wr[c * 5 + 0] * ip[0] + wr[c * 5 + 1] * ip[1] + wr[c * 5 + 2] * ip[2] +
+               wr[c * 5 + 3] * ip[3] + wr[c * 5 + 4] * ip[4];
+      }
+      o3[o * 44 + t2] = fmaxf(acc, 0.0f);
+    }
+    __syncthreads();
+    if (tid < 20) {
+      float m = o3[tid * 44];
+      for (int t2 = 1; t2 < 41; ++t2) m = fmaxf(m, o3[tid * 44 + t2]);
+      pooled[b2 * C_ + obase + tid] = m;
+    }
+    flag_signal(&flags[F_C3]);
+    return;
+  }
+
+  else if (bid < RB_PB) {
+    const int q = bid - RB_PW;
+    const int total = 2 * G4_ * KP_;
+    for (int idx = q * 256 + (int)threadIdx.x; idx < total; idx += NB_PW * 256) {
+      int d = idx / (G4_ * KP_);
+      int rem = idx % (G4_ * KP_);
+      int j = rem / KP_, k2 = rem % KP_;
+      const float* w2 = d ? w_ih_b : w_ih_f;
+      float v0 = 0.f, v1 = 0.f;
+      if (k2 < 200) { v0 = w2[(size_t)j * DHID_ + 2 * k2]; v1 = w2[(size_t)j * DHID_ + 2 * k2 + 1]; }
+      unsigned p0 = pack_split(v0), p1 = pack_split(v1);
+      apH[idx] = (p0 & 0xFFFFu) | (p1 << 16);
+      apL[idx] = (p0 >> 16) | (p1 & 0xFFFF0000u);
+    }
+    flag_signal(&flags[F_PW]);
+    return;
+  }
+
+  else if (bid < RB_GEMM) {
+    flag_wait(&flags[F_C3], NB_C3, 8);
+    const int q = bid - RB_PB;
+    const int tid = threadIdx.x;
+    if (tid < KP_) {
+      int k2 = tid;
+      for (int rr = 0; rr < 8; ++rr) {
+        int r = q * 8 + rr;
+        int t2 = r >> 5, b2 = r & 31;
+        float v0 = 0.f, v1 = 0.f;
+        if (k2 < 150) {
+          const float* e2 = word_emb + (size_t)x[b2 * S_ + t2] * E_;
+          v0 = e2[2 * k2]; v1 = e2[2 * k2 + 1];
+        } else if (k2 < 200) {
+          v0 = pooled[b2 * C_ + 2 * k2 - 300];
+          v1 = pooled[b2 * C_ + 2 * k2 - 299];
+        }
+        unsigned p0 = pack_split(v0), p1 = pack_split(v1);
+        bpH[(size_t)r * KP_ + k2] = (p0 & 0xFFFFu) | (p1 << 16);
+        bpL[(size_t)r * KP_ + k2] = (p0 >> 16) | (p1 & 0xFFFF0000u);
+      }
+    }
+    flag_signal(&flags[F_PB]);
+    return;
+  }
+
+  else if (bid < RB_FC) {
+    flag_wait(&flags[F_PW], NB_PW, 16);
+    flag_wait(&flags[F_PB], NB_PB, 16);
+    const int q = bid - RB_GEMM;
+    const int d = q & 1;
+    const int jt = (q >> 1) & 7;
+    const int rtb = q >> 4;
+    const int rt = d ? (31 - rtb) : rtb;
+    const int j0 = jt * 128, r0 = rt * 128;
+    const int tid = threadIdx.x;
+    const int w = tid >> 6, l = tid & 63;
+    const int lx = l & 15, lq = l >> 4;
+
+    unsigned* aH = sm.gemm.aH;
+    unsigned* aL = sm.gemm.aL;
+    unsigned* bH = sm.gemm.bH;
+    unsigned* bL = sm.gemm.bL;
+
+    f32x4 acch[2][8], accl[2][8];
+#pragma unroll
+    for (int mt = 0; mt < 2; ++mt)
+#pragma unroll
+      for (int nt = 0; nt < 8; ++nt) {
+        f32x4 z = {0.f, 0.f, 0.f, 0.f};
+        acch[mt][nt] = z; accl[mt][nt] = z;
+      }
+
+    const int jr = tid >> 1, hh = tid & 1;
+    const int q_st = jr >> 4, lane_lo = jr & 15;
+    const unsigned* arH = apH + ((size_t)(d * G4_ + j0 + jr)) * KP_ + hh * 8;
+    const unsigned* arL = apL + ((size_t)(d * G4_ + j0 + jr)) * KP_ + hh * 8;
+    const unsigned* brH = bpH + ((size_t)(r0 + jr)) * KP_ + hh * 8;
+    const unsigned* brL = bpL + ((size_t)(r0 + jr)) * KP_ + hh * 8;
+    const int w0 = (q_st * 64 + lane_lo + 32 * hh) * 4;
+    const int w1 = (q_st * 64 + lane_lo + 32 * hh + 16) * 4;
+
+    for (int Kt = 0; Kt < 13; ++Kt) {
+      uint4 a0 = *(const uint4*)(arH + Kt * 16);
+      uint4 a1 = *(const uint4*)(arH + Kt * 16 + 4);
+      uint4 c0v = *(const uint4*)(arL + Kt * 16);
+      uint4 c1v = *(const uint4*)(arL + Kt * 16 + 4);
+      uint4 e0 = *(const uint4*)(brH + Kt * 16);
+      uint4 e1 = *(const uint4*)(brH + Kt * 16 + 4);
+      uint4 f0 = *(const uint4*)(brL + Kt * 16);
+      uint4 f1 = *(const uint4*)(brL + Kt * 16 + 4);
+      *(uint4*)&aH[w0] = a0; *(uint4*)&aH[w1] = a1;
+      *(uint4*)&aL[w0] = c0v; *(uint4*)&aL[w1] = c1v;
+      *(uint4*)&bH[w0] = e0; *(uint4*)&bH[w1] = e1;
+      *(uint4*)&bL[w0] = f0; *(uint4*)&bL[w1] = f1;
+      __syncthreads();
+
+      union u4h { uint4 u; half8 h; };
+      u4h AH0, AH1, AL0, AL1;
+      AH0.u = *(const uint4*)&aH[((2 * w + 0) * 64 + l) * 4];
+      AH1.u = *(const uint4*)&aH[((2 * w + 1) * 64 + l) * 4];
+      AL0.u = *(const uint4*)&aL[((2 * w + 0) * 64 + l) * 4];
+      AL1.u = *(const uint4*)&aL[((2 * w + 1) * 64 + l) * 4];
+#pragma unroll
+      for (int nt = 0; nt < 8; ++nt) {
+        u4h BHn, BLn;
+        BHn.u = *(const uint4*)&bH[(nt * 64 + l) * 4];
+        BLn.u = *(const uint4*)&bL[(nt * 64 + l) * 4];
+        acch[0][nt] = __builtin_amdgcn_mfma_f32_16x16x32_f16(AH0.h, BHn.h, acch[0][nt], 0, 0, 0);
+        accl[0][nt] = __builtin_amdgcn_mfma_f32_16x16x32_f16(AH0.h, BLn.h, accl[0][nt], 0, 0, 0);
+        accl[0][nt] = __builtin_amdgcn_mfma_f32_16x16x32_f16(AL0.h, BHn.h, accl[0][nt], 0, 0, 0);
+        acch[1][nt] = __builtin_amdgcn_mfma_f32_16x16x32_f16(AH1.h, BHn.h, acch[1][nt], 0, 0, 0);
+        accl[1][nt] = __builtin_amdgcn_mfma_f32_16x16x32_f16(AH1.h, BLn.h, accl[1][nt], 0, 0, 0);
+        accl[1][nt] = __builtin_amdgcn_mfma_f32_16x16x32_f16(AL1.h, BHn.h, accl[1][nt], 0, 0, 0);
+      }
+      __syncthreads();
+    }
+
+    const float* bias = d ? b_b : b_f;
+    const float inv2048 = 1.0f / 2048.0f;
+#pragma unroll
+    for (int mt = 0; mt < 2; ++mt) {
+#pragma unroll
+      for (int nt = 0; nt < 8; ++nt) {
+        int rr = r0 + nt * 16 + lx;
+        int tt = rr >> 5, bb2 = rr & 31;
+        unsigned* dst = (unsigned*)gi + ((size_t)(d * S_ + tt) * G4_) * B_ + bb2;
+#pragma unroll
+        for (int r4 = 0; r4 < 4; ++r4) {
+          int j = j0 + (2 * w + mt) * 16 + lq * 4 + r4;
+          float vv = acch[mt][nt][r4] + accl[mt][nt][r4] * inv2048 + bias[j];
+          __hip_atomic_store(&dst[(size_t)j * B_], __builtin_bit_cast(unsigned, vv),
+                             __ATOMIC_RELAXED, __HIP_MEMORY_SCOPE_AGENT);
+        }
+      }
+    }
+    return;
+  }
+
+  else if (bid < RB_SMV) {
+    const int s = bid - RB_FC;
+    const int tid = threadIdx.x;
+    float* wT = sm.fc.wT;
+    float* psum = sm.fc.psum;
+    for (int i = tid; i < L_ * 512; i += 256) {
+      int l2 = i / 512, k = i % 512;
+      wT[k * 18 + l2] = fc_w[i];
+    }
+    const float* hf = hbuf + (size_t)(s + 1) * (H_ * B_);
+    const float* hbk = hbuf + (size_t)(S_ + 1 + (S_ - s)) * (H_ * B_);
+    const unsigned* hfu = (const unsigned*)hf;
+    const unsigned* hbku = (const unsigned*)hbk;
+    for (;;) {
+      unsigned a = __hip_atomic_load(&hfu[0], __ATOMIC_RELAXED, __HIP_MEMORY_SCOPE_AGENT);
+      unsigned c = __hip_atomic_load(&hbku[0], __ATOMIC_RELAXED, __HIP_MEMORY_SCOPE_AGENT);
+      if (a != SENTF_ && c != SENTF_) break;
+      __builtin_amdgcn_s_sleep(32);
+    }
+    const int b2 = tid & 31, kq = tid >> 5;
+    const unsigned* basep = (kq < 4) ? hfu : hbku;
+    const int koff = (kq < 4) ? kq * 64 : kq * 64 - 256;
+    unsigned hraw[64];
+    for (;;) {
+      bool pend = false;
+#pragma unroll
+      for (int i = 0; i < 64; ++i)
+        hraw[i] = __hip_atomic_load(&basep[(size_t)(koff + i) * 32 + b2],
+                                    __ATOMIC_RELAXED, __HIP_MEMORY_SCOPE_AGENT);
+#pragma unroll
+      for (int i = 0; i < 64; ++i) pend |= (hraw[i] == SENTF_);
+      if (!pend) break;
+      __builtin_amdgcn_s_sleep(8);
+    }
+    __syncthreads();
+    float acc[L_];
+#pragma unroll
+    for (int l2 = 0; l2 < L_; ++l2) acc[l2] = 0.f;
+#pragma unroll
+    for (int i = 0; i < 64; ++i) {
+      int k = kq * 64 + i;
+      float hv = __builtin_bit_cast(float, hraw[i]);
+      const float* wr = &wT[k * 18];
+#pragma unroll
+      for (int l2 = 0; l2 < L_; ++l2) acc[l2] = fmaf(hv, wr[l2], acc[l2]);
+    }
+#pragma unroll
+    for (int l2 = 0; l2 < L_; ++l2) psum[tid * 18 + l2] = acc[l2];
+    __syncthreads();
+    for (int idx = tid; idx < B_ * L_; idx += 256) {
+      int bb2 = idx & 31, l2 = idx >> 5;
+      float sum = fc_b[l2];
+      for (int q2 = 0; q2 < 8; ++q2) sum += psum[(q2 * 32 + bb2) * 18 + l2];
+      __hip_atomic_store((unsigned*)&em[((size_t)bb2 * S_ + s) * L_ + l2],
+                         __builtin_bit_cast(unsigned, sum),
+                         __ATOMIC_RELAXED, __HIP_MEMORY_SCOPE_AGENT);
+    }
+    return;
+  }
+
+  else {
+    const int bb = bid - RB_SMV;
+    const int tid = threadIdx.x;
+    float* e = sm.smv.e;
+    float* tr = sm.smv.tr;
+    auto sc = sm.smv.sc;
+    int* hist = sm.smv.hist;
+    int* tags = sm.smv.tags;
+
+    int ei[9];
+#pragma unroll
+    for (int j = 0; j < 9; ++j) { int i = tid + j * 256; ei[j] = (i < S_ * L_) ? i : tid; }
+    const unsigned* emu = (const unsigned*)em + (size_t)bb * S_ * L_;
+    unsigned ev[9];
+    for (;;) {
+      bool pend = false;
+#pragma unroll
+      for (int j = 0; j < 9; ++j)
+        ev[j] = __hip_atomic_load(&emu[ei[j]], __ATOMIC_RELAXED, __HIP_MEMORY_SCOPE_AGENT);
+#pragma unroll
+      for (int j = 0; j < 9; ++j) pend |= (ev[j] == SENTF_);
+      if (!pend) break;
+      __builtin_amdgcn_s_sleep(127);
+    }
+#pragma unroll
+    for (int j = 0; j < 9; ++j) e[ei[j]] = __builtin_bit_cast(float, ev[j]);
+    for (int i = tid; i < L_ * L_; i += 256) tr[i] = trans[i];
+    __syncthreads();
     if (tid < L_) {
-      int j = tid;
-      float ev = e[t * L_ + j];
+      int l2 = tid;
+      float m = -INFINITY;
+      for (int s2 = 0; s2 < S_; ++s2) m = fmaxf(m, e[s2 * L_ + l2]);
+      float sum2 = 0.f;
+      for (int s2 = 0; s2 < S_; ++s2) {
+        float ex = expf(e[s2 * L_ + l2] - m);
+        e[s2 * L_ + l2] = ex;
+        sum2 += ex;
+      }
+      for (int s2 = 0; s2 < S_; ++s2) e[s2 * L_ + l2] = e[s2 * L_ + l2] / sum2;
+    }
+    __syncthreads();
+    if (tid < L_) sc[0][tid] = start_t[tid] + e[tid];
+    __syncthreads();
+    int cbuf = 0;
+    for (int t2 = 1; t2 < S_; ++t2) {
+      if (tid < L_) {
+        int j2 = tid;
+        float evv = e[t2 * L_ + j2];
+        float best = -INFINITY;
+        int arg = 0;
+        for (int i = 0; i < L_; ++i) {
+          float v = (sc[cbuf][i] + tr[i * L_ + j2]) + evv;
+          if (v > best) { best = v; arg = i; }
+        }
+        int maskt = (x[bb * S_ + t2] != 0);
+        sc[cbuf ^ 1][j2] = maskt ? best : sc[cbuf][j2];
+        hist[(t2 - 1) * L_ + j2] = arg;
+      }
+      __syncthreads();
+      cbuf ^= 1;
+    }
+    if (tid == 0) {
       float best = -INFINITY;
-      int arg = 0;
-      for (int i = 0; i < L_; ++i) {
-        float v = (sc[cbuf][i] + tr[i * L_ + j]) + ev;
-        if (v > best) { best = v; arg = i; }
-      }
-      int maskt = (x[b * S_ + t] != 0);
-      sc[cbuf ^ 1][j] = maskt ? best : sc[cbuf][j];
-      hist[(t - 1) * L_ + j] = arg;
-    }
-    __syncthreads();
-    cbuf ^= 1;
-  }
-  if (tid == 0) {
-    float best = -INFINITY;
-    int last = 0;
-    for (int j = 0; j < L_; ++j) {
-      float v = sc[cbuf][j] + end_t[j];
-      if (v > best) { best = v; last = j; }
-    }
-    int cur = last;
-    tags[S_ - 1] = cur;
-    for (int p = S_ - 2; p >= 0; --p) {
-      if (x[b * S_ + p + 1] != 0) cur = hist[p * L_ + cur];
-      tags[p] = cur;
-    }
-  }
-  __syncthreads();
-  for (int s = tid; s < S_; s += 64) out[b * S_ + s] = tags[s];
+      int last = 0;
+      for (int j2 = 0; j2 < L_; ++j2) {
+        float v = sc[cbuf][j2] + end_t[j2];
+        if (v > best) { best = v; last = j2; }
+      }
+      int cur = last;
+      tags[S_ - 1] = cur;
+      for (int p = S_ - 2; p >= 0; --p) {
+        if (x[bb * S_ + p + 1] != 0) cur = hist[p * L_ + cur];
+        tags[p] = cur;
+      }
+    }
+    __syncthreads();
+    for (int s2 = tid; s2 < S_; s2 += 256) out[bb * S_ + s2] = tags[s2];
+    return;
+  }
 }
 
 extern "C" void kernel_launch(void* const* d_in, const int* in_sizes, int n_in,
@@ -603,16 +781,14 @@
   float* out1    = (float*)alloc(sizeof(float) * B_ * C_ * 48);
   float* out2    = (float*)alloc(sizeof(float) * B_ * C_ * 45);
   float* em      = (float*)alloc(sizeof(float) * B_ * S_ * L_);
-
-  const int hinit_total = 2 * (S_ + 1) * SLAB_;
-  k_hinit<<<(hinit_total + 255) / 256, 256, 0, stream>>>(h0, hfrag);
-  k_prep_w<<<(2 * G4_ * KP_ + 255) / 256, 256, 0, stream>>>(w_ih_f, w_ih_b, apH, apL);
-  k_conv1<<<dim3(32, 2), 256, 0, stream>>>(x_char, char_emb, conv1_w, conv1_b, out1);
-  k_conv2<<<dim3(32, 4), 256, 0, stream>>>(out1, conv2_w, conv2_b, out2);
-  k_conv3<<<dim3(32, 5), 256, 0, stream>>>(out2, conv3_w, conv3_b, pooled);
-  k_prep_b<<<4096, 256, 0, stream>>>(x, word_emb, pooled, bpH, bpL);
-  k_gemm<<<dim3(8, 32, 2), 256, 0, stream>>>(apH, apL, bpH, bpL, b_f, b_b, gi);
-  k_lstm<<<dim3(NBLKD, 2), 256, 0, stream>>>(w_hh_f, w_hh_b, c0, gi, hbuf, hfrag);
-  k_fc<<<S_, 256, 0, stream>>>(hbuf, fc_w, fc_b, em);
-  k_smv<<<B_, 64, 0, stream>>>(em, x, start_t, trans, end_t, out);
+  int* flags     = (int*)alloc(sizeof(int) * 16);
+
+  k_fill<<<2048, 256, 0, stream>>>(h0, hfrag, (unsigned*)hbuf, (unsigned*)gi,
+                                   (unsigned*)em, flags);
+  k_mega<<<NBLK_MEGA, 256, 0, stream>>>(
+      x, x_char, word_emb, char_emb,
+      conv1_w, conv1_b, conv2_w, conv2_b, conv3_w, conv3_b,
+      w_ih_f, w_ih_b, w_hh_f, w_hh_b, b_f, b_b, c0, fc_w, fc_b,
+      start_t, trans, end_t,
+      pooled, gi, hbuf, hfrag, apH, apL, bpH, bpL, out1, out2, em, flags, out);
 }
```

New measurement: 1.680 ms. 1.81x slower.
